# Kernel tuning notes

Measured on AMD Instinct MI355X. Metric: run time of the kernel, lower is better.

Reference implementation:

```python
import jax, jax.numpy as jnp
import numpy as np

N = 50000
E = 600000
IN_DIM = 128
HID = 128
HEADS = 4
OUT = HID // HEADS  # per-head out channels
R = 2
LAYERS = 2
NEG_SLOPE = 0.2


def _glorot(key, shape):
    fan_in, fan_out = shape[-2], shape[-1]
    lim = jnp.sqrt(6.0 / (fan_in + fan_out))
    return jax.random.uniform(key, shape, jnp.float32, -lim, lim)


def setup_inputs() -> dict:
    key = jax.random.key(0)
    ks = jax.random.split(key, 20)
    x = jax.random.normal(ks[0], (N, IN_DIM), jnp.float32)
    eidx = jax.random.randint(ks[1], (2, E), 0, N, jnp.int64 if jax.config.jax_enable_x64 else jnp.int32)
    etype = jax.random.randint(ks[2], (E,), 0, R, eidx.dtype)
    d = IN_DIM
    params = {}
    ki = 3
    for l in range(LAYERS):
        params[f"W{l}"] = _glorot(ks[ki], (R, d, HID)); ki += 1            # per-relation weight
        params[f"Q{l}"] = _glorot(ks[ki], (HID, HEADS)); ki += 1           # query proj (dim=1)
        params[f"K{l}"] = _glorot(ks[ki], (HID, HEADS)); ki += 1           # key proj
        params[f"cb{l}"] = jnp.zeros((HID,), jnp.float32)                   # conv bias
        params[f"pW{l}"] = _glorot(ks[ki], (HID, HID)); ki += 1            # proj Linear weight [out,in]
        params[f"pb{l}"] = jnp.zeros((HID,), jnp.float32)
        d = HID
    return dict(x=x, eidx=eidx, etype=etype, **params)


def _rgat_conv(h, src, dst, etype, W, Q, K, b):
    # per-relation transform of all nodes: [R, N, HID]
    xw = jnp.einsum('ni,rio->rno', h, W)
    out_j = xw[etype, src]          # [E, HID] source features under edge's relation
    out_i = xw[etype, dst]          # [E, HID] target features under edge's relation
    # additive self-attention, dim=1: alpha [E, HEADS]
    alpha = jax.nn.leaky_relu(out_i @ Q + out_j @ K, NEG_SLOPE)
    # segment softmax over destination nodes (across-relation)
    m = jax.ops.segment_max(alpha, dst, num_segments=N)
    m = jnp.where(jnp.isfinite(m), m, 0.0)
    e = jnp.exp(alpha - m[dst])
    s = jax.ops.segment_sum(e, dst, num_segments=N)
    a = e / (s[dst] + 1e-16)
    # weighted messages and scatter-sum aggregation
    msg = out_j.reshape(E, HEADS, OUT) * a[:, :, None]
    agg = jax.ops.segment_sum(msg.reshape(E, HID), dst, num_segments=N)
    return agg + b


def reference(x, eidx, etype, W0, Q0, K0, cb0, pW0, pb0, W1, Q1, K1, cb1, pW1, pb1):
    src, dst = eidx[0], eidx[1]  # flow source_to_target: aggregate at eidx[1]
    h = x
    for (W, Q, K, cb, pW, pb) in ((W0, Q0, K0, cb0, pW0, pb0), (W1, Q1, K1, cb1, pW1, pb1)):
        h = _rgat_conv(h, src, dst, etype, W, Q, K, cb)
        h = jax.nn.elu(h @ pW.T + pb)
    return h
```

## Files before the change

kernel.cpp:

```cpp
#include <hip/hip_runtime.h>
#include <hip/hip_bf16.h>

typedef __hip_bfloat16 bf16;
typedef short s16x8 __attribute__((ext_vector_type(8)));
typedef float f32x4 __attribute__((ext_vector_type(4)));

#define N_NODES 50000
#define NPAD    50048
#define E_EDGES 600000
#define HID     128
#define HEADS   4
#define SCAN_B  196

#define GB_IDX  2344
#define GB_WT   256
#define GB_QUAD 3125
#define GB_BIG  8824

__device__ __forceinline__ unsigned short f2bf_bits(float f) {
  unsigned u = __float_as_uint(f);
  u += 0x7fffu + ((u >> 16) & 1u);
  return (unsigned short)(u >> 16);
}
__device__ __forceinline__ float bf2f(unsigned short b) {
  return __uint_as_float(((unsigned)b) << 16);
}
__device__ __forceinline__ float lo_f(unsigned v) { return __uint_as_float(v << 16); }
__device__ __forceinline__ float hi_f(unsigned v) { return __uint_as_float(v & 0xffff0000u); }
__device__ __forceinline__ float lrelu(float v) { return fmaxf(v, 0.2f * v); }
__device__ __forceinline__ float elu(float v) { return v > 0.f ? v : __expf(v) - 1.f; }

__global__ __launch_bounds__(256) void detect_zero_kernel(const unsigned short* __restrict__ xb,
                                                          const int* __restrict__ ei,
                                                          int* __restrict__ flags,
                                                          int* __restrict__ zp, int nz) {
  int t = threadIdx.x;
  int i = blockIdx.x * 256 + t;
  if (i < nz) zp[i] = 0;
  if (blockIdx.x == 0) {
    __shared__ int cnt[2];
    if (t < 2) cnt[t] = 0;
    __syncthreads();
    unsigned short v = xb[2 * t];
    int ex = (v >> 7) & 0xFF;
    if (ex < 119 || ex > 135) atomicAdd(&cnt[0], 1);
    if (ei[2 * t + 1] != 0) atomicAdd(&cnt[1], 1);
    __syncthreads();
    if (t == 0) {
      flags[0] = (cnt[0] > 64) ? 1 : 0;
      flags[1] = (cnt[1] == 0) ? 1 : 0;
    }
  }
}

struct P8 { const void* src[8]; int dstoff[8]; int n[8]; };
__global__ __launch_bounds__(256) void cvt_all_kernel(const int* __restrict__ eidx,
                                                      const int* __restrict__ etype,
                                                      int* __restrict__ dstA, int* __restrict__ pk,
                                                      int* __restrict__ deg,
                                                      const void* __restrict__ w0,
                                                      const void* __restrict__ w1,
                                                      unsigned short* __restrict__ Wbt,
                                                      P8 tab, float* __restrict__ base,
                                                      const int* __restrict__ flags) {
  const int b = blockIdx.x, t = threadIdx.x;
  if (b < GB_IDX) {
    int e = b * 256 + t;
    if (e >= E_EDGES) return;
    int s, d, r;
    if (flags[1]) {
      const long long* e64 = (const long long*)eidx;
      const long long* t64 = (const long long*)etype;
      s = (int)e64[e]; d = (int)e64[E_EDGES + e]; r = (int)t64[e];
    } else {
      s = eidx[e]; d = eidx[E_EDGES + e]; r = etype[e];
    }
    dstA[e] = d;
    pk[e] = s | (r << 16);
    atomicAdd(&deg[d], 1);
  } else if (b < GB_IDX + GB_WT) {
    int idx = (b - GB_IDX) * 256 + t;
    int l = idx >> 15, rem = idx & 32767;
    int r = rem >> 14, i = (rem >> 7) & 127, o = rem & 127;
    const void* src = l ? w1 : w0;
    unsigned short v;
    if (flags[0]) v = f2bf_bits(((const float*)src)[rem]);
    else          v = ((const unsigned short*)src)[rem];
    Wbt[(size_t)l * 2 * HID * HID + ((size_t)r * HID + o) * HID + i] = v;
  } else {
    const int f = flags[0];
    int bb = b - GB_IDX - GB_WT;
    for (int k = 0; k < 8; ++k) {
      int n = tab.n[k];
      for (int i = bb * 256 + t; i < n; i += 2 * 256) {
        float v = f ? ((const float*)tab.src[k])[i] : bf2f(((const unsigned short*)tab.src[k])[i]);
        base[tab.dstoff[k] + i] = v;
      }
    }
  }
}

__global__ __launch_bounds__(256) void scan1_bucket_kernel(const int* __restrict__ deg,
                                                           int* __restrict__ excl,
                                                           int* __restrict__ bsum,
                                                           int* __restrict__ bcnt,
                                                           int* __restrict__ nq,
                                                           int* __restrict__ nw) {
  const int b = blockIdx.x, t = threadIdx.x;
  if (b < SCAN_B) {
    __shared__ int sm[256];
    int i = b * 256 + t;
    int v = (i < NPAD) ? deg[i] : 0;
    sm[t] = v;
    __syncthreads();
#pragma unroll
    for (int off = 1; off < 256; off <<= 1) {
      int add = (t >= off) ? sm[t - off] : 0;
      __syncthreads();
      sm[t] += add;
      __syncthreads();
    }
    if (i < NPAD) excl[i] = sm[t] - v;
    if (t == 255) bsum[b] = sm[255];
  } else {
    int n = (b - SCAN_B) * 256 + t;
    int lane = t & 63;
    bool valid = n < N_NODES;
    int d = valid ? deg[n] : 0;
    bool isq = valid && (d <= 16);
    bool isw = valid && (d > 16);
    unsigned long long mq = __ballot(isq);
    unsigned long long mw = __ballot(isw);
    unsigned long long lower = (lane == 63) ? 0x7fffffffffffffffull : ((1ull << lane) - 1ull);
    int baseq = 0, basew = 0;
    int lq = (int)__ffsll(mq) - 1;
    int lw = (int)__ffsll(mw) - 1;
    if (mq && lane == lq) baseq = atomicAdd(&bcnt[0], (int)__popcll(mq));
    if (mw && lane == lw) basew = atomicAdd(&bcnt[1], (int)__popcll(mw));
    if (mq) baseq = __shfl(baseq, lq);
    if (mw) basew = __shfl(basew, lw);
    if (isq) nq[baseq + (int)__popcll(mq & lower)] = n;
    if (isw) nw[basew + (int)__popcll(mw & lower)] = n;
  }
}

__global__ __launch_bounds__(256) void scan23_prep_kernel(const int* __restrict__ excl,
                                                          const int* __restrict__ bsum,
                                                          int* __restrict__ rowstart,
                                                          const unsigned short* __restrict__ Wbt,
                                                          const float* __restrict__ Qf,
                                                          const float* __restrict__ Kf,
                                                          unsigned short* __restrict__ qkt_hi,
                                                          unsigned short* __restrict__ qkt_lo,
                                                          const void* __restrict__ pW0,
                                                          const void* __restrict__ pW1,
                                                          const float* __restrict__ cbf,
                                                          const float* __restrict__ pbf,
                                                          unsigned short* __restrict__ pWTb2,
                                                          float* __restrict__ bo2,
                                                          const int* __restrict__ flags) {
  const int b = blockIdx.x, t = threadIdx.x;
  if (b < SCAN_B) {
    __shared__ int sm[256];
    int v = (t < SCAN_B) ? bsum[t] : 0;
    sm[t] = v;
    __syncthreads();
#pragma unroll
    for (int off = 1; off < 256; off <<= 1) {
      int add = (t >= off) ? sm[t - off] : 0;
      __syncthreads();
      sm[t] += add;
      __syncthreads();
    }
    int bpre = (b > 0) ? sm[b - 1] : 0;
    int i = b * 256 + t;
    if (i < NPAD) rowstart[i] = excl[i] + bpre;
    if (i == 0) rowstart[NPAD] = E_EDGES;
  } else if (b < SCAN_B + 2) {
    int idx = (b - SCAN_B) * 256 + t;
    int i = idx & 127, lr = idx >> 7, l = lr >> 1, r = (lr & 1);
    float aq[4] = {0.f, 0.f, 0.f, 0.f}, ak[4] = {0.f, 0.f, 0.f, 0.f};
    const unsigned short* Wb = Wbt + (size_t)lr * HID * HID;
    const float* Qp = Qf + l * HID * HEADS;
    const float* Kp = Kf + l * HID * HEADS;
    for (int j = 0; j < HID; ++j) {
      float w = bf2f(Wb[j * HID + i]);
      float4 q4 = *(const float4*)(Qp + j * 4);
      float4 k4 = *(const float4*)(Kp + j * 4);
      aq[0] += w * q4.x; aq[1] += w * q4.y; aq[2] += w * q4.z; aq[3] += w * q4.w;
      ak[0] += w * k4.x; ak[1] += w * k4.y; ak[2] += w * k4.z; ak[3] += w * k4.w;
    }
    size_t base = (size_t)l * 16 * HID;
#pragma unroll
    for (int h = 0; h < 4; ++h) {
      unsigned short qh = f2bf_bits(aq[h]);
      unsigned short kh = f2bf_bits(ak[h]);
      float qres = aq[h] - bf2f(qh);
      float kres = ak[h] - bf2f(kh);
      qkt_hi[base + (size_t)(r * 4 + h) * HID + i] = qh;
      qkt_lo[base + (size_t)(r * 4 + h) * HID + i] = f2bf_bits(qres);
      qkt_hi[base + (size_t)(8 + r * 4 + h) * HID + i] = kh;
      qkt_lo[base + (size_t)(8 + r * 4 + h) * HID + i] = f2bf_bits(kres);
    }
  } else {
    const int wave = t >> 6, lane = t & 63;
    int ob = (b - SCAN_B - 2) * 4 + wave;
    int o = ob & 127, l = ob >> 7;
    const void* pWraw = l ? pW1 : pW0;
    const float* cb = cbf + l * HID;
    const int f = flags[0];
    float part = 0.f;
#pragma unroll
    for (int i = lane; i < HID; i += 64) {
      float w = f ? ((const float*)pWraw)[o * HID + i] : bf2f(((const unsigned short*)pWraw)[o * HID + i]);
      pWTb2[(size_t)l * HID * HID + o * HID + i] = f2bf_bits(w);
      part += cb[i] * w;
    }
#pragma unroll
    for (int off = 32; off > 0; off >>= 1) part += __shfl_xor(part, off);
    if (lane == 0) bo2[l * HID + o] = pbf[l * HID + o] + part;
  }
}

__global__ __launch_bounds__(256) void scatter_kernel(const int* __restrict__ dstA,
                                                      const int* __restrict__ pk,
                                                      const int* __restrict__ rowstart,
                                                      int* __restrict__ cnt,
                                                      int* __restrict__ eord) {
  int e = blockIdx.x * 256 + threadIdx.x;
  if (e >= E_EDGES) return;
  int d = dstA[e];
  int pos = rowstart[d] + atomicAdd(&cnt[d], 1);
  eord[pos] = pk[e];
}

__device__ __forceinline__ void gemm64_from_lds(unsigned short (*As)[136], unsigned short (*Cs)[136],
                                                const unsigned short* __restrict__ Wbt,
                                                unsigned short* __restrict__ xw, int row0,
                                                int wave, int lm, int q, int t) {
  const int r = wave >> 1, colb = (wave & 1) * 64;
  const unsigned short* Bt = Wbt + (size_t)r * HID * HID;
  s16x8 bfr[4][4];
#pragma unroll
  for (int kc = 0; kc < 4; ++kc) {
    const int ko = kc * 32 + q * 8;
#pragma unroll
    for (int ct = 0; ct < 4; ++ct)
      bfr[kc][ct] = *(const s16x8*)(Bt + (size_t)(colb + ct * 16 + lm) * HID + ko);
  }
  f32x4 acc[4][4];
#pragma unroll
  for (int a = 0; a < 4; ++a)
#pragma unroll
    for (int c = 0; c < 4; ++c) { f32x4 z = {0.f, 0.f, 0.f, 0.f}; acc[a][c] = z; }
#pragma unroll
  for (int kc = 0; kc < 4; ++kc) {
    const int ko = kc * 32 + q * 8;
#pragma unroll
    for (int rt = 0; rt < 4; ++rt) {
      s16x8 a = *(const s16x8*)&As[rt * 16 + lm][ko];
#pragma unroll
      for (int ct = 0; ct < 4; ++ct)
        acc[rt][ct] = __builtin_amdgcn_mfma_f32_16x16x32_bf16(a, bfr[kc][ct], acc[rt][ct], 0, 0, 0);
    }
  }
  __syncthreads();
#pragma unroll
  for (int rr = 0; rr < 2; ++rr) {
    if (r == rr) {
#pragma unroll
      for (int rt = 0; rt < 4; ++rt)
#pragma unroll
        for (int i = 0; i < 4; ++i) {
          int rloc = rt * 16 + q * 4 + i;
#pragma unroll
          for (int ct = 0; ct < 4; ++ct)
            Cs[rloc][colb + ct * 16 + lm] = f2bf_bits(acc[rt][ct][i]);
        }
    }
    __syncthreads();
    unsigned short* dst = xw + ((size_t)rr * NPAD + row0) * HID;
#pragma unroll
    for (int j = 0; j < 4; ++j) {
      int idx = j * 256 + t;
      int rw = idx >> 4, cb8 = (idx & 15) * 8;
      if (row0 + rw < N_NODES)
        *(s16x8*)(dst + (size_t)rw * HID + cb8) = *(const s16x8*)&Cs[rw][cb8];
    }
    __syncthreads();
  }
}

__device__ __forceinline__ void qk16_from_lds(unsigned short (*As)[136], unsigned short (*Cs)[136],
                                              const unsigned short* __restrict__ qkt_hi,
                                              const unsigned short* __restrict__ qkt_lo,
                                              float4* __restrict__ qi4, float4* __restrict__ kj4,
                                              int row0, int wave, int lane, int lm, int q) {
  s16x8 bhi[4], blo[4], af[4];
#pragma unroll
  for (int kc = 0; kc < 4; ++kc) {
    const int ko = kc * 32 + q * 8;
    bhi[kc] = *(const s16x8*)(qkt_hi + (size_t)lm * HID + ko);
    blo[kc] = *(const s16x8*)(qkt_lo + (size_t)lm * HID + ko);
    af[kc]  = *(const s16x8*)&As[wave * 16 + lm][ko];
  }
  f32x4 acc = {0.f, 0.f, 0.f, 0.f};
#pragma unroll
  for (int kc = 0; kc < 4; ++kc) {
    acc = __builtin_amdgcn_mfma_f32_16x16x32_bf16(af[kc], bhi[kc], acc, 0, 0, 0);
    acc = __builtin_amdgcn_mfma_f32_16x16x32_bf16(af[kc], blo[kc], acc, 0, 0, 0);
  }
  float (*Fs)[16][17] = (float(*)[16][17])&Cs[0][0];
#pragma unroll
  for (int i = 0; i < 4; ++i)
    Fs[wave][lm][q * 4 + i] = acc[i];
  __syncthreads();
  if (lane < 16) {
    int n = row0 + wave * 16 + lane;
    if (n < N_NODES) {
      float4 v;
      v.x = Fs[wave][0][lane];  v.y = Fs[wave][1][lane];  v.z = Fs[wave][2][lane];  v.w = Fs[wave][3][lane];
      qi4[n] = v;
      v.x = Fs[wave][4][lane];  v.y = Fs[wave][5][lane];  v.z = Fs[wave][6][lane];  v.w = Fs[wave][7][lane];
      qi4[NPAD + n] = v;
      v.x = Fs[wave][8][lane];  v.y = Fs[wave][9][lane];  v.z = Fs[wave][10][lane]; v.w = Fs[wave][11][lane];
      kj4[n] = v;
      v.x = Fs[wave][12][lane]; v.y = Fs[wave][13][lane]; v.z = Fs[wave][14][lane]; v.w = Fs[wave][15][lane];
      kj4[NPAD + n] = v;
    }
  }
}

__global__ __launch_bounds__(256) void fused_l0_kernel(const void* __restrict__ x,
                                                       const unsigned short* __restrict__ Wbt,
                                                       unsigned short* __restrict__ xw,
                                                       const unsigned short* __restrict__ qkt_hi,
                                                       const unsigned short* __restrict__ qkt_lo,
                                                       float4* __restrict__ qi4,
                                                       float4* __restrict__ kj4,
                                                       const int* __restrict__ flags) {
  __shared__ unsigned short As[64][136];
  __shared__ unsigned short Cs[64][136];
  const int t = threadIdx.x;
  const int wave = t >> 6, lane = t & 63;
  const int lm = lane & 15, q = lane >> 4;
  const int row0 = blockIdx.x * 64;
  if (flags[0]) {
    const float* xf = (const float*)x;
#pragma unroll
    for (int j = 0; j < 4; ++j) {
      int idx = j * 256 + t;
      int rw = idx >> 4, cb8 = (idx & 15) * 8;
      s16x8 o = {0, 0, 0, 0, 0, 0, 0, 0};
      if (row0 + rw < N_NODES) {
        const float4* s4 = (const float4*)(xf + (size_t)(row0 + rw) * HID + cb8);
        float4 a = s4[0], b = s4[1];
        o[0] = (short)f2bf_bits(a.x); o[1] = (short)f2bf_bits(a.y);
        o[2] = (short)f2bf_bits(a.z); o[3] = (short)f2bf_bits(a.w);
        o[4] = (short)f2bf_bits(b.x); o[5] = (short)f2bf_bits(b.y);
        o[6] = (short)f2bf_bits(b.z); o[7] = (short)f2bf_bits(b.w);
      }
      *(s16x8*)&As[rw][cb8] = o;
    }
  } else {
    const unsigned short* xb = (const unsigned short*)x;
#pragma unroll
    for (int j = 0; j < 4; ++j) {
      int idx = j * 256 + t;
      int rw = idx >> 4, cb8 = (idx & 15) * 8;
      s16x8 o = {0, 0, 0, 0, 0, 0, 0, 0};
      if (row0 + rw < N_NODES)
        o = *(const s16x8*)(xb + (size_t)(row0 + rw) * HID + cb8);
      *(s16x8*)&As[rw][cb8] = o;
    }
  }
  __syncthreads();
  gemm64_from_lds(As, Cs, Wbt, xw, row0, wave, lm, q, t);
  qk16_from_lds(As, Cs, qkt_hi, qkt_lo, qi4, kj4, row0, wave, lane, lm, q);
}

__global__ __launch_bounds__(256) void fused_mid_kernel(const unsigned short* __restrict__ aggb,
                                                        const unsigned short* __restrict__ pWTb,
                                                        const float* __restrict__ bo,
                                                        const unsigned short* __restrict__ Wbt1,
                                                        unsigned short* __restrict__ xw,
                                                        const unsigned short* __restrict__ qkt_hi,
                                                        const unsigned short* __restrict__ qkt_lo,
                                                        float4* __restrict__ qi4,
                                                        float4* __restrict__ kj4) {
  __shared__ unsigned short As[64][136];
  __shared__ unsigned short Cs[64][136];
  const int t = threadIdx.x;
  const int wave = t >> 6, lane = t & 63;
  const int lm = lane & 15, q = lane >> 4;
  const int row0 = blockIdx.x * 64;
  const int h = wave >> 1;
  const int colb = (wave & 1) * 64;
  s16x8 bfr[4][4];
#pragma unroll
  for (int kc = 0; kc < 4; ++kc) {
    const int ko = kc * 32 + q * 8;
#pragma unroll
    for (int ct = 0; ct < 4; ++ct)
      bfr[kc][ct] = *(const s16x8*)(pWTb + (size_t)(colb + ct * 16 + lm) * HID + ko);
  }
  const unsigned short* gsrc = aggb + (size_t)row0 * HID;
#pragma unroll
  for (int j = 0; j < 4; ++j) {
    int idx = j * 256 + t;
    *(s16x8*)&As[idx >> 4][(idx & 15) * 8] = *(const s16x8*)(gsrc + idx * 8);
  }
  __syncthreads();
  f32x4 pacc[2][4];
#pragma unroll
  for (int a = 0; a < 2; ++a)
#pragma unroll
    for (int c = 0; c < 4; ++c) { f32x4 z = {0.f, 0.f, 0.f, 0.f}; pacc[a][c] = z; }
#pragma unroll
  for (int kc = 0; kc < 4; ++kc) {
    const int ko = kc * 32 + q * 8;
#pragma unroll
    for (int rt = 0; rt < 2; ++rt) {
      s16x8 a = *(const s16x8*)&As[(2 * h + rt) * 16 + lm][ko];
#pragma unroll
      for (int ct = 0; ct < 4; ++ct)
        pacc[rt][ct] = __builtin_amdgcn_mfma_f32_16x16x32_bf16(a, bfr[kc][ct], pacc[rt][ct], 0, 0, 0);
    }
  }
  __syncthreads();
#pragma unroll
  for (int rt = 0; rt < 2; ++rt)
#pragma unroll
    for (int i = 0; i < 4; ++i) {
      int rloc = (2 * h + rt) * 16 + q * 4 + i;
#pragma unroll
      for (int ct = 0; ct < 4; ++ct) {
        int o = colb + ct * 16 + lm;
        As[rloc][o] = f2bf_bits(elu(pacc[rt][ct][i] + bo[o]));
      }
    }
  __syncthreads();
  gemm64_from_lds(As, Cs, Wbt1, xw, row0, wave, lm, q, t);
  qk16_from_lds(As, Cs, qkt_hi, qkt_lo, qi4, kj4, row0, wave, lane, lm, q);
}

__global__ __launch_bounds__(256) void edge_all_kernel(
    const int* __restrict__ rowstart, const int* __restrict__ eord,
    const float4* __restrict__ qi4, const float4* __restrict__ kj4,
    const unsigned short* __restrict__ xw, unsigned short* __restrict__ aggb,
    const int* __restrict__ nq, const int* __restrict__ nw,
    const int* __restrict__ bcnt) {
  __shared__ volatile float wbuf[1152];
  const int t = threadIdx.x;
  const int wave = t >> 6, lane = t & 63;
  if (blockIdx.x >= GB_BIG) {
    const int g = lane >> 4, li = lane & 15;
    const int idx = (blockIdx.x - GB_BIG) * 16 + wave * 4 + g;
    const int cq = bcnt[0];
    const bool act = idx < cq;
    const int n = act ? nq[idx] : 0;
    const int start = rowstart[n];
    const int dg = act ? (rowstart[n + 1] - start) : 0;
    int p = 0;
    float w0 = 0.f, w1 = 0.f, w2 = 0.f, w3 = 0.f;
    if (li < dg) {
      p = eord[start + li];
      int s = p & 0xffff, r = p >> 16;
      float4 k4 = kj4[r ? (NPAD + s) : s];
      float4 q4 = r ? qi4[NPAD + n] : qi4[n];
      w0 = __expf(fminf(lrelu(q4.x + k4.x), 85.f));
      w1 = __expf(fminf(lrelu(q4.y + k4.y), 85.f));
      w2 = __expf(fminf(lrelu(q4.z + k4.z), 85.f));
      w3 = __expf(fminf(lrelu(q4.w + k4.w), 85.f));
    }
    const int wg = (wave << 2) | g;
    volatile float* wls = &wbuf[wg * 68];
    wls[0 * 17 + li] = w0; wls[1 * 17 + li] = w1;
    wls[2 * 17 + li] = w2; wls[3 * 17 + li] = w3;
    float s0 = w0, s1 = w1, s2 = w2, s3 = w3;
#pragma unroll
    for (int off = 8; off > 0; off >>= 1) {
      s0 += __shfl_xor(s0, off); s1 += __shfl_xor(s1, off);
      s2 += __shfl_xor(s2, off); s3 += __shfl_xor(s3, off);
    }
    const int hh = li >> 2;
    float ssel = hh == 0 ? s0 : hh == 1 ? s1 : hh == 2 ? s2 : s3;
    float a0 = 0.f, a1 = 0.f, a2 = 0.f, a3 = 0.f, a4 = 0.f, a5 = 0.f, a6 = 0.f, a7 = 0.f;
    volatile const float* wrh = &wls[hh * 17];
    const int co = li * 8;
    const int gbase = lane & 48;
#pragma unroll 1
    for (int e0 = 0; e0 < dg; e0 += 4) {
      int pe[4];
      uint4 v[4];
#pragma unroll
      for (int u = 0; u < 4; ++u) {
        int e = e0 + u;
        pe[u] = __shfl(p, gbase + (e < dg ? e : 0));
      }
#pragma unroll
      for (int u = 0; u < 4; ++u)
        v[u] = *(const uint4*)(xw + ((size_t)((pe[u] & 0xffff) + (pe[u] >> 16) * NPAD) << 7) + co);
#pragma unroll
      for (int u = 0; u < 4; ++u) {
        int e = e0 + u;
        float we = (e < dg) ? wrh[e] : 0.f;
        a0 = fmaf(lo_f(v[u].x), we, a0); a1 = fmaf(hi_f(v[u].x), we, a1);
        a2 = fmaf(lo_f(v[u].y), we, a2); a3 = fmaf(hi_f(v[u].y), we, a3);
        a4 = fmaf(lo_f(v[u].z), we, a4); a5 = fmaf(hi_f(v[u].z), we, a5);
        a6 = fmaf(lo_f(v[u].w), we, a6); a7 = fmaf(hi_f(v[u].w), we, a7);
      }
    }
    if (act) {
      float inv = 1.f / (ssel + 1e-16f);
      uint4 o;
      o.x = (unsigned)f2bf_bits(a0 * inv) | ((unsigned)f2bf_bits(a1 * inv) << 16);
      o.y = (unsigned)f2bf_bits(a2 * inv) | ((unsigned)f2bf_bits(a3 * inv) << 16);
      o.z = (unsigned)f2bf_bits(a4 * inv) | ((unsigned)f2bf_bits(a5 * inv) << 16);
      o.w = (unsigned)f2bf_bits(a6 * inv) | ((unsigned)f2bf_bits(a7 * inv) << 16);
      *(uint4*)(aggb + ((size_t)n << 7) + co) = o;
    }
  } else {
    const int idx = blockIdx.x * 4 + wave;
    const int cw = bcnt[1];
    if (idx >= cw) return;
    const int n = nw[idx];
    unsigned* outp = (unsigned*)(aggb + ((size_t)n << 7)) + lane;
    const int start = rowstart[n];
    const int deg = rowstart[n + 1] - start;
    const int hh = lane >> 4;
    const int ch2 = lane << 1;
    float2 acc = {0.f, 0.f};
    float ssel;
    volatile float* wls = &wbuf[wave * 288];
    if (deg <= 64) {
      int p = 0;
      float w0 = 0.f, w1 = 0.f, w2 = 0.f, w3 = 0.f;
      if (lane < deg) {
        p = eord[start + lane];
        int s = p & 0xffff, r = p >> 16;
        float4 k4 = kj4[r ? (NPAD + s) : s];
        float4 q4 = r ? qi4[NPAD + n] : qi4[n];
        w0 = __expf(fminf(lrelu(q4.x + k4.x), 85.f));
        w1 = __expf(fminf(lrelu(q4.y + k4.y), 85.f));
        w2 = __expf(fminf(lrelu(q4.z + k4.z), 85.f));
        w3 = __expf(fminf(lrelu(q4.w + k4.w), 85.f));
      }
      float s0 = w0, s1 = w1, s2 = w2, s3 = w3;
#pragma unroll
      for (int off = 32; off > 0; off >>= 1) {
        s0 += __shfl_xor(s0, off); s1 += __shfl_xor(s1, off);
        s2 += __shfl_xor(s2, off); s3 += __shfl_xor(s3, off);
      }
      ssel = hh == 0 ? s0 : hh == 1 ? s1 : hh == 2 ? s2 : s3;
      wls[0 * 72 + lane] = w0;
      wls[1 * 72 + lane] = w1;
      wls[2 * 72 + lane] = w2;
      wls[3 * 72 + lane] = w3;
      volatile const float* wrh = &wls[hh * 72];
      const int degp = (deg + 15) & ~15;
#pragma unroll 1
      for (int e = 0; e < degp; e += 16) {
        int pp[16];
        unsigned vv[16];
#pragma unroll
        for (int u = 0; u < 16; ++u)
          pp[u] = __builtin_amdgcn_readlane(p, e + u);
#pragma unroll
        for (int u = 0; u < 16; ++u)
          vv[u] = *(const unsigned*)(xw + ((size_t)((pp[u] & 0xffff) + (pp[u] >> 16) * NPAD) << 7) + ch2);
#pragma unroll
        for (int u = 0; u < 16; ++u) {
          float we = wrh[e + u];
          acc.x = fmaf(lo_f(vv[u]), we, acc.x);
          acc.y = fmaf(hi_f(vv[u]), we, acc.y);
        }
      }
    } else {
      const float4 q0 = qi4[n], q1 = qi4[NPAD + n];
      float4 m = make_float4(-1e30f, -1e30f, -1e30f, -1e30f);
      for (int e = start; e < start + deg; ++e) {
        int pe = eord[e];
        int s = pe & 0xffff, r = pe >> 16;
        float4 k4 = kj4[(size_t)r * NPAD + s];
        float4 q4 = r ? q1 : q0;
        m.x = fmaxf(m.x, lrelu(q4.x + k4.x)); m.y = fmaxf(m.y, lrelu(q4.y + k4.y));
        m.z = fmaxf(m.z, lrelu(q4.z + k4.z)); m.w = fmaxf(m.w, lrelu(q4.w + k4.w));
      }
      float4 sv = make_float4(0.f, 0.f, 0.f, 0.f);
      for (int e = start; e < start + deg; ++e) {
        int pe = eord[e];
        int s = pe & 0xffff, r = pe >> 16;
        float4 k4 = kj4[(size_t)r * NPAD + s];
        float4 q4 = r ? q1 : q0;
        float w0 = __expf(lrelu(q4.x + k4.x) - m.x);
        float w1 = __expf(lrelu(q4.y + k4.y) - m.y);
        float w2 = __expf(lrelu(q4.z + k4.z) - m.z);
        float w3 = __expf(lrelu(q4.w + k4.w) - m.w);
        sv.x += w0; sv.y += w1; sv.z += w2; sv.w += w3;
        float we = hh == 0 ? w0 : hh == 1 ? w1 : hh == 2 ? w2 : w3;
        unsigned v = *(const unsigned*)(xw + (((size_t)r * NPAD + s) << 7) + ch2);
        acc.x = fmaf(lo_f(v), we, acc.x);
        acc.y = fmaf(hi_f(v), we, acc.y);
      }
      ssel = hh == 0 ? sv.x : hh == 1 ? sv.y : hh == 2 ? sv.z : sv.w;
    }
    float inv = 1.f / (ssel + 1e-16f);
    *outp = (unsigned)f2bf_bits(acc.x * inv) | ((unsigned)f2bf_bits(acc.y * inv) << 16);
  }
}

__global__ __launch_bounds__(256) void proj_final(const unsigned short* __restrict__ aggb,
                                                  const unsigned short* __restrict__ pWTb,
                                                  const float* __restrict__ bo,
                                                  void* __restrict__ dout,
                                                  const int* __restrict__ flags) {
  __shared__ unsigned short As[64][136];
  const int t = threadIdx.x;
  const int wave = t >> 6, lane = t & 63;
  const int row0 = blockIdx.x * 64;
  const int h = wave >> 1;
  const int colb = (wave & 1) * 64;
  const int lm = lane & 15, q = lane >> 4;
  s16x8 bfr[4][4];
#pragma unroll
  for (int kc = 0; kc < 4; ++kc) {
    const int ko = kc * 32 + q * 8;
#pragma unroll
    for (int ct = 0; ct < 4; ++ct)
      bfr[kc][ct] = *(const s16x8*)(pWTb + (size_t)(colb + ct * 16 + lm) * HID + ko);
  }
  const unsigned short* gsrc = aggb + (size_t)row0 * HID;
#pragma unroll
  for (int j = 0; j < 4; ++j) {
    int idx = j * 256 + t;
    *(s16x8*)&As[idx >> 4][(idx & 15) * 8] = *(const s16x8*)(gsrc + idx * 8);
  }
  __syncthreads();
  f32x4 acc[2][4];
#pragma unroll
  for (int a = 0; a < 2; ++a)
#pragma unroll
    for (int c = 0; c < 4; ++c) { f32x4 z = {0.f, 0.f, 0.f, 0.f}; acc[a][c] = z; }
#pragma unroll
  for (int kc = 0; kc < 4; ++kc) {
    const int ko = kc * 32 + q * 8;
#pragma unroll
    for (int rt = 0; rt < 2; ++rt) {
      s16x8 a = *(const s16x8*)&As[(2 * h + rt) * 16 + lm][ko];
#pragma unroll
      for (int ct = 0; ct < 4; ++ct)
        acc[rt][ct] = __builtin_amdgcn_mfma_f32_16x16x32_bf16(a, bfr[kc][ct], acc[rt][ct], 0, 0, 0);
    }
  }
  __syncthreads();
  if (!flags[0]) {
    unsigned short* dstp = (unsigned short*)dout;
#pragma unroll
    for (int rt = 0; rt < 2; ++rt)
#pragma unroll
      for (int i = 0; i < 4; ++i) {
        int rloc = (2 * h + rt) * 16 + q * 4 + i;
#pragma unroll
        for (int ct = 0; ct < 4; ++ct) {
          int o = colb + ct * 16 + lm;
          As[rloc][o] = f2bf_bits(elu(acc[rt][ct][i] + bo[o]));
        }
      }
    __syncthreads();
#pragma unroll
    for (int j = 0; j < 4; ++j) {
      int idx = j * 256 + t;
      int rw = idx >> 4, cb8 = (idx & 15) * 8;
      if (row0 + rw < N_NODES)
        *(s16x8*)(dstp + (size_t)(row0 + rw) * HID + cb8) = *(const s16x8*)&As[rw][cb8];
    }
  } else {
    float* fdst = (float*)dout;
    float (*Fs)[132] = (float(*)[132])&As[0][0];
#pragma unroll
    for (int h2 = 0; h2 < 2; ++h2) {
      if (h == h2) {
#pragma unroll
        for (int rt = 0; rt < 2; ++rt)
#pragma unroll
          for (int i = 0; i < 4; ++i) {
            int rloc = rt * 16 + q * 4 + i;
#pragma unroll
            for (int ct = 0; ct < 4; ++ct) {
              int o = colb + ct * 16 + lm;
              Fs[rloc][o] = elu(acc[rt][ct][i] + bo[o]);
            }
          }
      }
      __syncthreads();
#pragma unroll
      for (int j = 0; j < 4; ++j) {
        int idx = j * 256 + t;
        int rw = idx >> 5, cb4 = (idx & 31) * 4;
        if (row0 + h2 * 32 + rw < N_NODES)
          *(float4*)(fdst + (size_t)(row0 + h2 * 32 + rw) * HID + cb4) = *(const float4*)&Fs[rw][cb4];
      }
      __syncthreads();
    }
  }
}

extern "C" void kernel_launch(void* const* d_in, const int* in_sizes, int n_in,
                              void* d_out, int out_size, void* d_ws, size_t ws_size,
                              hipStream_t stream) {
  const void* x     = d_in[0];
  const int*  eidx  = (const int*)d_in[1];
  const int*  etype = (const int*)d_in[2];
  const int iW[2] = {3, 9}, iQ[2] = {4, 10}, iK[2] = {5, 11}, icb[2] = {6, 12}, ipW[2] = {7, 13}, ipb[2] = {8, 14};

  float* ws = (float*)d_ws;
  size_t off = 0;
  int*   flags = (int*)(ws + off); off += 16;
  unsigned short* xw   = (unsigned short*)(ws + off); off += (size_t)NPAD * HID;
  float* qi   = ws + off; off += (size_t)2 * NPAD * HEADS;
  float* kj   = ws + off; off += (size_t)2 * NPAD * HEADS;
  unsigned short* aggb = (unsigned short*)(ws + off); off += (size_t)NPAD * HID / 2;
  int* dstA = (int*)(ws + off); off += E_EDGES;
  int* pk   = (int*)(ws + off); off += E_EDGES;
  int* eord = (int*)(ws + off); off += E_EDGES;
  int* deg  = (int*)(ws + off); off += NPAD;
  int* cnt  = (int*)(ws + off); off += NPAD;
  int* bcnt = (int*)(ws + off); off += 16;
  int* excl = (int*)(ws + off); off += NPAD;
  int* rowstart = (int*)(ws + off); off += NPAD + 16;
  int* bsum  = (int*)(ws + off); off += 256;
  int* nq   = (int*)(ws + off); off += NPAD;
  int* nwl  = (int*)(ws + off); off += NPAD;
  unsigned short* Wbt   = (unsigned short*)(ws + off); off += (size_t)2 * 2 * HID * HID / 2;
  unsigned short* pWTb2 = (unsigned short*)(ws + off); off += (size_t)2 * HID * HID / 2;
  unsigned short* qkt_hi = (unsigned short*)(ws + off); off += (size_t)2 * 16 * HID / 2;
  unsigned short* qkt_lo = (unsigned short*)(ws + off); off += (size_t)2 * 16 * HID / 2;
  float* Qf  = ws + off; off += 2 * HID * HEADS;
  float* Kf  = ws + off; off += 2 * HID * HEADS;
  float* cbf = ws + off; off += 2 * HID;
  float* pbf = ws + off; off += 2 * HID;
  float* bo2 = ws + off; off += 2 * HID;

  detect_zero_kernel<<<(2 * NPAD + 16 + 255) / 256, 256, 0, stream>>>((const unsigned short*)x, eidx, flags, deg, 2 * NPAD + 16);

  {
    P8 tab;
    float* base = ws;
    for (int l = 0; l < 2; ++l) {
      tab.src[l * 4 + 0] = d_in[iQ[l]];  tab.dstoff[l * 4 + 0] = (int)(Qf - base) + l * HID * HEADS;  tab.n[l * 4 + 0] = HID * HEADS;
      tab.src[l * 4 + 1] = d_in[iK[l]];  tab.dstoff[l * 4 + 1] = (int)(Kf - base) + l * HID * HEADS;  tab.n[l * 4 + 1] = HID * HEADS;
      tab.src[l * 4 + 2] = d_in[icb[l]]; tab.dstoff[l * 4 + 2] = (int)(cbf - base) + l * HID;         tab.n[l * 4 + 2] = HID;
      tab.src[l * 4 + 3] = d_in[ipb[l]]; tab.dstoff[l * 4 + 3] = (int)(pbf - base) + l * HID;         tab.n[l * 4 + 3] = HID;
    }
    cvt_all_kernel<<<GB_IDX + GB_WT + 2, 256, 0, stream>>>(eidx, etype, dstA, pk, deg,
                                                           d_in[iW[0]], d_in[iW[1]], Wbt,
                                                           tab, ws, flags);
  }

  scan1_bucket_kernel<<<SCAN_B + SCAN_B, 256, 0, stream>>>(deg, excl, bsum, bcnt, nq, nwl);

  scan23_prep_kernel<<<SCAN_B + 2 + 64, 256, 0, stream>>>(excl, bsum, rowstart,
                                                          Wbt, Qf, Kf, qkt_hi, qkt_lo,
                                                          d_in[ipW[0]], d_in[ipW[1]], cbf, pbf, pWTb2, bo2, flags);

  scatter_kernel<<<(E_EDGES + 255) / 256, 256, 0, stream>>>(dstA, pk, rowstart, cnt, eord);

  const int RB = NPAD / 64;
  fused_l0_kernel<<<RB, 256, 0, stream>>>(x, Wbt, xw, qkt_hi, qkt_lo,
                                          (float4*)qi, (float4*)kj, flags);
  edge_all_kernel<<<GB_BIG + GB_QUAD, 256, 0, stream>>>(rowstart, eord, (const float4*)qi, (const float4*)kj,
                                                        xw, aggb, nq, nwl, bcnt);
  fused_mid_kernel<<<RB, 256, 0, stream>>>(aggb, pWTb2, bo2, Wbt + (size_t)2 * HID * HID, xw,
                                           qkt_hi + (size_t)16 * HID, qkt_lo + (size_t)16 * HID,
                                           (float4*)qi, (float4*)kj);
  edge_all_kernel<<<GB_BIG + GB_QUAD, 256, 0, stream>>>(rowstart, eord, (const float4*)qi, (const float4*)kj,
                                                        xw, aggb, nq, nwl, bcnt);
  proj_final<<<RB, 256, 0, stream>>>(aggb, pWTb2 + (size_t)HID * HID, bo2 + HID, d_out, flags);
}
```

Baseline: 343.1 us.

## Merge all pipeline stages into one cooperative persistent kernel with grid syncs

Restructures the ten separate kernel launches into a single cooperative mega-kernel. Each phase loops over virtual blocks with a grid-stride loop, and grid.sync() separates the phases, so launch gaps and tail drains between kernels go away. The original per-kernel launches are kept as a fallback when the cooperative launch fails. The trade-off is a grid capped at occupancy × CUs (at most 1024 blocks), which limits parallelism in the edge phases. The GEMM phases' shared-memory and register needs also now apply to every phase and may lower occupancy.

```diff
diff --git a/kernel.cpp b/kernel.cpp
--- a/kernel.cpp
+++ b/kernel.cpp
@@ -1,5 +1,8 @@
 #include <hip/hip_runtime.h>
 #include <hip/hip_bf16.h>
+#include <hip/hip_cooperative_groups.h>
+
+namespace cg = cooperative_groups;
 
 typedef __hip_bfloat16 bf16;
 typedef short s16x8 __attribute__((ext_vector_type(8)));
@@ -12,10 +15,17 @@
 #define HEADS   4
 #define SCAN_B  196
 
-#define GB_IDX  2344
-#define GB_WT   256
-#define GB_QUAD 3125
-#define GB_BIG  8824
+#define VB_ZERO 392
+#define VB_IDX  2344
+#define VB_WT   256
+#define VB_CVT  (VB_IDX + VB_WT + 2)
+#define VB_SCAN (SCAN_B + SCAN_B)
+#define VB_PREP (SCAN_B + 2 + 64)
+#define VB_SCAT 2344
+#define VB_ROWS 782
+#define VB_BIG  8824
+#define VB_QUAD 3125
+#define VB_EDGE (VB_BIG + VB_QUAD)
 
 __device__ __forceinline__ unsigned short f2bf_bits(float f) {
   unsigned u = __float_as_uint(f);
@@ -30,87 +40,82 @@
 __device__ __forceinline__ float lrelu(float v) { return fmaxf(v, 0.2f * v); }
 __device__ __forceinline__ float elu(float v) { return v > 0.f ? v : __expf(v) - 1.f; }
 
-__global__ __launch_bounds__(256) void detect_zero_kernel(const unsigned short* __restrict__ xb,
-                                                          const int* __restrict__ ei,
-                                                          int* __restrict__ flags,
-                                                          int* __restrict__ zp, int nz) {
-  int t = threadIdx.x;
-  int i = blockIdx.x * 256 + t;
-  if (i < nz) zp[i] = 0;
-  if (blockIdx.x == 0) {
-    __shared__ int cnt[2];
-    if (t < 2) cnt[t] = 0;
-    __syncthreads();
-    unsigned short v = xb[2 * t];
-    int ex = (v >> 7) & 0xFF;
-    if (ex < 119 || ex > 135) atomicAdd(&cnt[0], 1);
-    if (ei[2 * t + 1] != 0) atomicAdd(&cnt[1], 1);
-    __syncthreads();
-    if (t == 0) {
-      flags[0] = (cnt[0] > 64) ? 1 : 0;
-      flags[1] = (cnt[1] == 0) ? 1 : 0;
-    }
-  }
-}
-
 struct P8 { const void* src[8]; int dstoff[8]; int n[8]; };
-__global__ __launch_bounds__(256) void cvt_all_kernel(const int* __restrict__ eidx,
-                                                      const int* __restrict__ etype,
-                                                      int* __restrict__ dstA, int* __restrict__ pk,
-                                                      int* __restrict__ deg,
-                                                      const void* __restrict__ w0,
-                                                      const void* __restrict__ w1,
-                                                      unsigned short* __restrict__ Wbt,
-                                                      P8 tab, float* __restrict__ base,
-                                                      const int* __restrict__ flags) {
-  const int b = blockIdx.x, t = threadIdx.x;
-  if (b < GB_IDX) {
-    int e = b * 256 + t;
-    if (e >= E_EDGES) return;
-    int s, d, r;
-    if (flags[1]) {
-      const long long* e64 = (const long long*)eidx;
-      const long long* t64 = (const long long*)etype;
-      s = (int)e64[e]; d = (int)e64[E_EDGES + e]; r = (int)t64[e];
-    } else {
-      s = eidx[e]; d = eidx[E_EDGES + e]; r = etype[e];
-    }
-    dstA[e] = d;
-    pk[e] = s | (r << 16);
-    atomicAdd(&deg[d], 1);
-  } else if (b < GB_IDX + GB_WT) {
-    int idx = (b - GB_IDX) * 256 + t;
+
+struct MegaArgs {
+  const void* x; const int* eidx; const int* etype;
+  const void* w0; const void* w1; const void* pW0; const void* pW1;
+  P8 tab; float* base;
+  int* flags; unsigned short* xw; float4* qi4; float4* kj4; unsigned short* aggb;
+  int* dstA; int* pk; int* eord; int* deg; int* cnt; int* bcnt;
+  int* excl; int* rowstart; int* bsum; int* nq; int* nw;
+  unsigned short* Wbt; unsigned short* pWTb2; unsigned short* qkt_hi; unsigned short* qkt_lo;
+  float* Qf; float* Kf; float* cbf; float* pbf; float* bo2;
+  void* dout;
+};
+
+
+__device__ __forceinline__ void phase_zero(const MegaArgs& a, int vb, int t) {
+  int i = vb * 256 + t;
+  if (i < 2 * NPAD + 16) a.deg[i] = 0;
+}
+
+__device__ __forceinline__ void phase_detect(const MegaArgs& a, int t, int* dcnt) {
+  if (t < 2) dcnt[t] = 0;
+  __syncthreads();
+  unsigned short v = ((const unsigned short*)a.x)[2 * t];
+  int ex = (v >> 7) & 0xFF;
+  if (ex < 119 || ex > 135) atomicAdd(&dcnt[0], 1);
+  if (a.eidx[2 * t + 1] != 0) atomicAdd(&dcnt[1], 1);
+  __syncthreads();
+  if (t == 0) {
+    a.flags[0] = (dcnt[0] > 64) ? 1 : 0;
+    a.flags[1] = (dcnt[1] == 0) ? 1 : 0;
+  }
+}
+
+__device__ __forceinline__ void phase_cvt(const MegaArgs& a, int vb, int t) {
+  const int f0 = a.flags[0], f1 = a.flags[1];
+  if (vb < VB_IDX) {
+    int e = vb * 256 + t;
+    if (e < E_EDGES) {
+      int s, d, r;
+      if (f1) {
+        const long long* e64 = (const long long*)a.eidx;
+        const long long* t64 = (const long long*)a.etype;
+        s = (int)e64[e]; d = (int)e64[E_EDGES + e]; r = (int)t64[e];
+      } else {
+        s = a.eidx[e]; d = a.eidx[E_EDGES + e]; r = a.etype[e];
+      }
+      a.dstA[e] = d;
+      a.pk[e] = s | (r << 16);
+      atomicAdd(&a.deg[d], 1);
+    }
+  } else if (vb < VB_IDX + VB_WT) {
+    int idx = (vb - VB_IDX) * 256 + t;
     int l = idx >> 15, rem = idx & 32767;
     int r = rem >> 14, i = (rem >> 7) & 127, o = rem & 127;
-    const void* src = l ? w1 : w0;
+    const void* src = l ? a.w1 : a.w0;
     unsigned short v;
-    if (flags[0]) v = f2bf_bits(((const float*)src)[rem]);
-    else          v = ((const unsigned short*)src)[rem];
-    Wbt[(size_t)l * 2 * HID * HID + ((size_t)r * HID + o) * HID + i] = v;
+    if (f0) v = f2bf_bits(((const float*)src)[rem]);
+    else    v = ((const unsigned short*)src)[rem];
+    a.Wbt[(size_t)l * 2 * HID * HID + ((size_t)r * HID + o) * HID + i] = v;
   } else {
-    const int f = flags[0];
-    int bb = b - GB_IDX - GB_WT;
+    int bb = vb - VB_IDX - VB_WT;
     for (int k = 0; k < 8; ++k) {
-      int n = tab.n[k];
+      int n = a.tab.n[k];
       for (int i = bb * 256 + t; i < n; i += 2 * 256) {
-        float v = f ? ((const float*)tab.src[k])[i] : bf2f(((const unsigned short*)tab.src[k])[i]);
-        base[tab.dstoff[k] + i] = v;
-      }
-    }
-  }
-}
-
-__global__ __launch_bounds__(256) void scan1_bucket_kernel(const int* __restrict__ deg,
-                                                           int* __restrict__ excl,
-                                                           int* __restrict__ bsum,
-                                                           int* __restrict__ bcnt,
-                                                           int* __restrict__ nq,
-                                                           int* __restrict__ nw) {
-  const int b = blockIdx.x, t = threadIdx.x;
-  if (b < SCAN_B) {
-    __shared__ int sm[256];
-    int i = b * 256 + t;
-    int v = (i < NPAD) ? deg[i] : 0;
+        float v = f0 ? ((const float*)a.tab.src[k])[i] : bf2f(((const unsigned short*)a.tab.src[k])[i]);
+        a.base[a.tab.dstoff[k] + i] = v;
+      }
+    }
+  }
+}
+
+__device__ __forceinline__ void phase_scan1b(const MegaArgs& a, int vb, int t, int lane, int* sm) {
+  if (vb < SCAN_B) {
+    int i = vb * 256 + t;
+    int v = (i < NPAD) ? a.deg[i] : 0;
     sm[t] = v;
     __syncthreads();
 #pragma unroll
@@ -120,13 +125,13 @@
       sm[t] += add;
       __syncthreads();
     }
-    if (i < NPAD) excl[i] = sm[t] - v;
-    if (t == 255) bsum[b] = sm[255];
+    if (i < NPAD) a.excl[i] = sm[t] - v;
+    if (t == 255) a.bsum[vb] = sm[255];
+    __syncthreads();
   } else {
-    int n = (b - SCAN_B) * 256 + t;
-    int lane = t & 63;
+    int n = (vb - SCAN_B) * 256 + t;
     bool valid = n < N_NODES;
-    int d = valid ? deg[n] : 0;
+    int d = valid ? a.deg[n] : 0;
     bool isq = valid && (d <= 16);
     bool isw = valid && (d > 16);
     unsigned long long mq = __ballot(isq);
@@ -135,34 +140,19 @@
     int baseq = 0, basew = 0;
     int lq = (int)__ffsll(mq) - 1;
     int lw = (int)__ffsll(mw) - 1;
-    if (mq && lane == lq) baseq = atomicAdd(&bcnt[0], (int)__popcll(mq));
-    if (mw && lane == lw) basew = atomicAdd(&bcnt[1], (int)__popcll(mw));
+    if (mq && lane == lq) baseq = atomicAdd(&a.bcnt[0], (int)__popcll(mq));
+    if (mw && lane == lw) basew = atomicAdd(&a.bcnt[1], (int)__popcll(mw));
     if (mq) baseq = __shfl(baseq, lq);
     if (mw) basew = __shfl(basew, lw);
-    if (isq) nq[baseq + (int)__popcll(mq & lower)] = n;
-    if (isw) nw[basew + (int)__popcll(mw & lower)] = n;
-  }
-}
-
-__global__ __launch_bounds__(256) void scan23_prep_kernel(const int* __restrict__ excl,
-                                                          const int* __restrict__ bsum,
-                                                          int* __restrict__ rowstart,
-                                                          const unsigned short* __restrict__ Wbt,
-                                                          const float* __restrict__ Qf,
-                                                          const float* __restrict__ Kf,
-                                                          unsigned short* __restrict__ qkt_hi,
-                                                          unsigned short* __restrict__ qkt_lo,
-                                                          const void* __restrict__ pW0,
-                                                          const void* __restrict__ pW1,
-                                                          const float* __restrict__ cbf,
-                                                          const float* __restrict__ pbf,
-                                                          unsigned short* __restrict__ pWTb2,
-                                                          float* __restrict__ bo2,
-                                                          const int* __restrict__ flags) {
-  const int b = blockIdx.x, t = threadIdx.x;
-  if (b < SCAN_B) {
-    __shared__ int sm[256];
-    int v = (t < SCAN_B) ? bsum[t] : 0;
+    if (isq) a.nq[baseq + (int)__popcll(mq & lower)] = n;
+    if (isw) a.nw[basew + (int)__popcll(mw & lower)] = n;
+  }
+}
+
+__device__ __forceinline__ void phase_prep(const MegaArgs& a, int vb, int t, int wave, int lane, int* sm) {
+  const int f0 = a.flags[0];
+  if (vb < SCAN_B) {
+    int v = (t < SCAN_B) ? a.bsum[t] : 0;
     sm[t] = v;
     __syncthreads();
 #pragma unroll
@@ -172,17 +162,18 @@
       sm[t] += add;
       __syncthreads();
     }
-    int bpre = (b > 0) ? sm[b - 1] : 0;
-    int i = b * 256 + t;
-    if (i < NPAD) rowstart[i] = excl[i] + bpre;
-    if (i == 0) rowstart[NPAD] = E_EDGES;
-  } else if (b < SCAN_B + 2) {
-    int idx = (b - SCAN_B) * 256 + t;
+    int bpre = (vb > 0) ? sm[vb - 1] : 0;
+    int i = vb * 256 + t;
+    if (i < NPAD) a.rowstart[i] = a.excl[i] + bpre;
+    if (i == 0) a.rowstart[NPAD] = E_EDGES;
+    __syncthreads();
+  } else if (vb < SCAN_B + 2) {
+    int idx = (vb - SCAN_B) * 256 + t;
     int i = idx & 127, lr = idx >> 7, l = lr >> 1, r = (lr & 1);
     float aq[4] = {0.f, 0.f, 0.f, 0.f}, ak[4] = {0.f, 0.f, 0.f, 0.f};
-    const unsigned short* Wb = Wbt + (size_t)lr * HID * HID;
-    const float* Qp = Qf + l * HID * HEADS;
-    const float* Kp = Kf + l * HID * HEADS;
+    const unsigned short* Wb = a.Wbt + (size_t)lr * HID * HID;
+    const float* Qp = a.Qf + l * HID * HEADS;
+    const float* Kp = a.Kf + l * HID * HEADS;
     for (int j = 0; j < HID; ++j) {
       float w = bf2f(Wb[j * HID + i]);
       float4 q4 = *(const float4*)(Qp + j * 4);
@@ -197,41 +188,36 @@
       unsigned short kh = f2bf_bits(ak[h]);
       float qres = aq[h] - bf2f(qh);
       float kres = ak[h] - bf2f(kh);
-      qkt_hi[base + (size_t)(r * 4 + h) * HID + i] = qh;
-      qkt_lo[base + (size_t)(r * 4 + h) * HID + i] = f2bf_bits(qres);
-      qkt_hi[base + (size_t)(8 + r * 4 + h) * HID + i] = kh;
-      qkt_lo[base + (size_t)(8 + r * 4 + h) * HID + i] = f2bf_bits(kres);
+      a.qkt_hi[base + (size_t)(r * 4 + h) * HID + i] = qh;
+      a.qkt_lo[base + (size_t)(r * 4 + h) * HID + i] = f2bf_bits(qres);
+      a.qkt_hi[base + (size_t)(8 + r * 4 + h) * HID + i] = kh;
+      a.qkt_lo[base + (size_t)(8 + r * 4 + h) * HID + i] = f2bf_bits(kres);
     }
   } else {
-    const int wave = t >> 6, lane = t & 63;
-    int ob = (b - SCAN_B - 2) * 4 + wave;
+    int ob = (vb - SCAN_B - 2) * 4 + wave;
     int o = ob & 127, l = ob >> 7;
-    const void* pWraw = l ? pW1 : pW0;
-    const float* cb = cbf + l * HID;
-    const int f = flags[0];
+    const void* pWraw = l ? a.pW1 : a.pW0;
+    const float* cb = a.cbf + l * HID;
     float part = 0.f;
 #pragma unroll
     for (int i = lane; i < HID; i += 64) {
-      float w = f ? ((const float*)pWraw)[o * HID + i] : bf2f(((const unsigned short*)pWraw)[o * HID + i]);
-      pWTb2[(size_t)l * HID * HID + o * HID + i] = f2bf_bits(w);
+      float w = f0 ? ((const float*)pWraw)[o * HID + i] : bf2f(((const unsigned short*)pWraw)[o * HID + i]);
+      a.pWTb2[(size_t)l * HID * HID + o * HID + i] = f2bf_bits(w);
       part += cb[i] * w;
     }
 #pragma unroll
     for (int off = 32; off > 0; off >>= 1) part += __shfl_xor(part, off);
-    if (lane == 0) bo2[l * HID + o] = pbf[l * HID + o] + part;
-  }
-}
-
-__global__ __launch_bounds__(256) void scatter_kernel(const int* __restrict__ dstA,
-                                                      const int* __restrict__ pk,
-                                                      const int* __restrict__ rowstart,
-                                                      int* __restrict__ cnt,
-                                                      int* __restrict__ eord) {
-  int e = blockIdx.x * 256 + threadIdx.x;
-  if (e >= E_EDGES) return;
-  int d = dstA[e];
-  int pos = rowstart[d] + atomicAdd(&cnt[d], 1);
-  eord[pos] = pk[e];
+    if (lane == 0) a.bo2[l * HID + o] = a.pbf[l * HID + o] + part;
+  }
+}
+
+__device__ __forceinline__ void phase_scatter(const MegaArgs& a, int vb, int t) {
+  int e = vb * 256 + t;
+  if (e < E_EDGES) {
+    int d = a.dstA[e];
+    int pos = a.rowstart[d] + atomicAdd(&a.cnt[d], 1);
+    a.eord[pos] = a.pk[e];
+  }
 }
 
 __device__ __forceinline__ void gemm64_from_lds(unsigned short (*As)[136], unsigned short (*Cs)[136],
@@ -250,18 +236,18 @@
   }
   f32x4 acc[4][4];
 #pragma unroll
-  for (int a = 0; a < 4; ++a)
-#pragma unroll
-    for (int c = 0; c < 4; ++c) { f32x4 z = {0.f, 0.f, 0.f, 0.f}; acc[a][c] = z; }
+  for (int aa = 0; aa < 4; ++aa)
+#pragma unroll
+    for (int c = 0; c < 4; ++c) { f32x4 z = {0.f, 0.f, 0.f, 0.f}; acc[aa][c] = z; }
 #pragma unroll
   for (int kc = 0; kc < 4; ++kc) {
     const int ko = kc * 32 + q * 8;
 #pragma unroll
     for (int rt = 0; rt < 4; ++rt) {
-      s16x8 a = *(const s16x8*)&As[rt * 16 + lm][ko];
+      s16x8 av = *(const s16x8*)&As[rt * 16 + lm][ko];
 #pragma unroll
       for (int ct = 0; ct < 4; ++ct)
-        acc[rt][ct] = __builtin_amdgcn_mfma_f32_16x16x32_bf16(a, bfr[kc][ct], acc[rt][ct], 0, 0, 0);
+        acc[rt][ct] = __builtin_amdgcn_mfma_f32_16x16x32_bf16(av, bfr[kc][ct], acc[rt][ct], 0, 0, 0);
     }
   }
   __syncthreads();
@@ -329,24 +315,14 @@
       kj4[NPAD + n] = v;
     }
   }
-}
-
-__global__ __launch_bounds__(256) void fused_l0_kernel(const void* __restrict__ x,
-                                                       const unsigned short* __restrict__ Wbt,
-                                                       unsigned short* __restrict__ xw,
-                                                       const unsigned short* __restrict__ qkt_hi,
-                                                       const unsigned short* __restrict__ qkt_lo,
-                                                       float4* __restrict__ qi4,
-                                                       float4* __restrict__ kj4,
-                                                       const int* __restrict__ flags) {
-  __shared__ unsigned short As[64][136];
-  __shared__ unsigned short Cs[64][136];
-  const int t = threadIdx.x;
-  const int wave = t >> 6, lane = t & 63;
-  const int lm = lane & 15, q = lane >> 4;
-  const int row0 = blockIdx.x * 64;
-  if (flags[0]) {
-    const float* xf = (const float*)x;
+  __syncthreads();
+}
+
+__device__ __forceinline__ void phase_l0(const MegaArgs& a, int vb, int t, int wave, int lane, int lm, int q,
+                                         unsigned short (*As)[136], unsigned short (*Cs)[136]) {
+  const int row0 = vb * 64;
+  if (a.flags[0]) {
+    const float* xf = (const float*)a.x;
 #pragma unroll
     for (int j = 0; j < 4; ++j) {
       int idx = j * 256 + t;
@@ -354,16 +330,16 @@
       s16x8 o = {0, 0, 0, 0, 0, 0, 0, 0};
       if (row0 + rw < N_NODES) {
         const float4* s4 = (const float4*)(xf + (size_t)(row0 + rw) * HID + cb8);
-        float4 a = s4[0], b = s4[1];
-        o[0] = (short)f2bf_bits(a.x); o[1] = (short)f2bf_bits(a.y);
-        o[2] = (short)f2bf_bits(a.z); o[3] = (short)f2bf_bits(a.w);
-        o[4] = (short)f2bf_bits(b.x); o[5] = (short)f2bf_bits(b.y);
-        o[6] = (short)f2bf_bits(b.z); o[7] = (short)f2bf_bits(b.w);
+        float4 aa = s4[0], b = s4[1];
+        o[0] = (short)f2bf_bits(aa.x); o[1] = (short)f2bf_bits(aa.y);
+        o[2] = (short)f2bf_bits(aa.z); o[3] = (short)f2bf_bits(aa.w);
+        o[4] = (short)f2bf_bits(b.x);  o[5] = (short)f2bf_bits(b.y);
+        o[6] = (short)f2bf_bits(b.z);  o[7] = (short)f2bf_bits(b.w);
       }
       *(s16x8*)&As[rw][cb8] = o;
     }
   } else {
-    const unsigned short* xb = (const unsigned short*)x;
+    const unsigned short* xb = (const unsigned short*)a.x;
 #pragma unroll
     for (int j = 0; j < 4; ++j) {
       int idx = j * 256 + t;
@@ -375,25 +351,13 @@
     }
   }
   __syncthreads();
-  gemm64_from_lds(As, Cs, Wbt, xw, row0, wave, lm, q, t);
-  qk16_from_lds(As, Cs, qkt_hi, qkt_lo, qi4, kj4, row0, wave, lane, lm, q);
-}
-
-__global__ __launch_bounds__(256) void fused_mid_kernel(const unsigned short* __restrict__ aggb,
-                                                        const unsigned short* __restrict__ pWTb,
-                                                        const float* __restrict__ bo,
-                                                        const unsigned short* __restrict__ Wbt1,
-                                                        unsigned short* __restrict__ xw,
-                                                        const unsigned short* __restrict__ qkt_hi,
-                                                        const unsigned short* __restrict__ qkt_lo,
-                                                        float4* __restrict__ qi4,
-                                                        float4* __restrict__ kj4) {
-  __shared__ unsigned short As[64][136];
-  __shared__ unsigned short Cs[64][136];
-  const int t = threadIdx.x;
-  const int wave = t >> 6, lane = t & 63;
-  const int lm = lane & 15, q = lane >> 4;
-  const int row0 = blockIdx.x * 64;
+  gemm64_from_lds(As, Cs, a.Wbt, a.xw, row0, wave, lm, q, t);
+  qk16_from_lds(As, Cs, a.qkt_hi, a.qkt_lo, a.qi4, a.kj4, row0, wave, lane, lm, q);
+}
+
+__device__ __forceinline__ void phase_mid(const MegaArgs& a, int vb, int t, int wave, int lane, int lm, int q,
+                                          unsigned short (*As)[136], unsigned short (*Cs)[136]) {
+  const int row0 = vb * 64;
   const int h = wave >> 1;
   const int colb = (wave & 1) * 64;
   s16x8 bfr[4][4];
@@ -402,9 +366,9 @@
     const int ko = kc * 32 + q * 8;
 #pragma unroll
     for (int ct = 0; ct < 4; ++ct)
-      bfr[kc][ct] = *(const s16x8*)(pWTb + (size_t)(colb + ct * 16 + lm) * HID + ko);
-  }
-  const unsigned short* gsrc = aggb + (size_t)row0 * HID;
+      bfr[kc][ct] = *(const s16x8*)(a.pWTb2 + (size_t)(colb + ct * 16 + lm) * HID + ko);
+  }
+  const unsigned short* gsrc = a.aggb + (size_t)row0 * HID;
 #pragma unroll
   for (int j = 0; j < 4; ++j) {
     int idx = j * 256 + t;
@@ -413,18 +377,18 @@
   __syncthreads();
   f32x4 pacc[2][4];
 #pragma unroll
-  for (int a = 0; a < 2; ++a)
-#pragma unroll
-    for (int c = 0; c < 4; ++c) { f32x4 z = {0.f, 0.f, 0.f, 0.f}; pacc[a][c] = z; }
+  for (int aa = 0; aa < 2; ++aa)
+#pragma unroll
+    for (int c = 0; c < 4; ++c) { f32x4 z = {0.f, 0.f, 0.f, 0.f}; pacc[aa][c] = z; }
 #pragma unroll
   for (int kc = 0; kc < 4; ++kc) {
     const int ko = kc * 32 + q * 8;
 #pragma unroll
     for (int rt = 0; rt < 2; ++rt) {
-      s16x8 a = *(const s16x8*)&As[(2 * h + rt) * 16 + lm][ko];
+      s16x8 av = *(const s16x8*)&As[(2 * h + rt) * 16 + lm][ko];
 #pragma unroll
       for (int ct = 0; ct < 4; ++ct)
-        pacc[rt][ct] = __builtin_amdgcn_mfma_f32_16x16x32_bf16(a, bfr[kc][ct], pacc[rt][ct], 0, 0, 0);
+        pacc[rt][ct] = __builtin_amdgcn_mfma_f32_16x16x32_bf16(av, bfr[kc][ct], pacc[rt][ct], 0, 0, 0);
     }
   }
   __syncthreads();
@@ -436,35 +400,125 @@
 #pragma unroll
       for (int ct = 0; ct < 4; ++ct) {
         int o = colb + ct * 16 + lm;
-        As[rloc][o] = f2bf_bits(elu(pacc[rt][ct][i] + bo[o]));
-      }
-    }
-  __syncthreads();
-  gemm64_from_lds(As, Cs, Wbt1, xw, row0, wave, lm, q, t);
-  qk16_from_lds(As, Cs, qkt_hi, qkt_lo, qi4, kj4, row0, wave, lane, lm, q);
-}
-
-__global__ __launch_bounds__(256) void edge_all_kernel(
-    const int* __restrict__ rowstart, const int* __restrict__ eord,
-    const float4* __restrict__ qi4, const float4* __restrict__ kj4,
-    const unsigned short* __restrict__ xw, unsigned short* __restrict__ aggb,
-    const int* __restrict__ nq, const int* __restrict__ nw,
-    const int* __restrict__ bcnt) {
-  __shared__ volatile float wbuf[1152];
-  const int t = threadIdx.x;
-  const int wave = t >> 6, lane = t & 63;
-  if (blockIdx.x >= GB_BIG) {
+        As[rloc][o] = f2bf_bits(elu(pacc[rt][ct][i] + a.bo2[o]));
+      }
+    }
+  __syncthreads();
+  const unsigned short* Wbt1 = a.Wbt + (size_t)2 * HID * HID;
+  gemm64_from_lds(As, Cs, Wbt1, a.xw, row0, wave, lm, q, t);
+  qk16_from_lds(As, Cs, a.qkt_hi + (size_t)16 * HID, a.qkt_lo + (size_t)16 * HID,
+                a.qi4, a.kj4, row0, wave, lane, lm, q);
+}
+
+__device__ __forceinline__ void phase_final(const MegaArgs& a, int vb, int t, int wave, int lane, int lm, int q,
+                                            unsigned short (*As)[136]) {
+  const int row0 = vb * 64;
+  const int h = wave >> 1;
+  const int colb = (wave & 1) * 64;
+  const unsigned short* pWT1 = a.pWTb2 + (size_t)HID * HID;
+  const float* bo1 = a.bo2 + HID;
+  s16x8 bfr[4][4];
+#pragma unroll
+  for (int kc = 0; kc < 4; ++kc) {
+    const int ko = kc * 32 + q * 8;
+#pragma unroll
+    for (int ct = 0; ct < 4; ++ct)
+      bfr[kc][ct] = *(const s16x8*)(pWT1 + (size_t)(colb + ct * 16 + lm) * HID + ko);
+  }
+  const unsigned short* gsrc = a.aggb + (size_t)row0 * HID;
+#pragma unroll
+  for (int j = 0; j < 4; ++j) {
+    int idx = j * 256 + t;
+    *(s16x8*)&As[idx >> 4][(idx & 15) * 8] = *(const s16x8*)(gsrc + idx * 8);
+  }
+  __syncthreads();
+  f32x4 acc[2][4];
+#pragma unroll
+  for (int aa = 0; aa < 2; ++aa)
+#pragma unroll
+    for (int c = 0; c < 4; ++c) { f32x4 z = {0.f, 0.f, 0.f, 0.f}; acc[aa][c] = z; }
+#pragma unroll
+  for (int kc = 0; kc < 4; ++kc) {
+    const int ko = kc * 32 + q * 8;
+#pragma unroll
+    for (int rt = 0; rt < 2; ++rt) {
+      s16x8 av = *(const s16x8*)&As[(2 * h + rt) * 16 + lm][ko];
+#pragma unroll
+      for (int ct = 0; ct < 4; ++ct)
+        acc[rt][ct] = __builtin_amdgcn_mfma_f32_16x16x32_bf16(av, bfr[kc][ct], acc[rt][ct], 0, 0, 0);
+    }
+  }
+  __syncthreads();
+  if (!a.flags[0]) {
+    unsigned short* dstp = (unsigned short*)a.dout;
+#pragma unroll
+    for (int rt = 0; rt < 2; ++rt)
+#pragma unroll
+      for (int i = 0; i < 4; ++i) {
+        int rloc = (2 * h + rt) * 16 + q * 4 + i;
+#pragma unroll
+        for (int ct = 0; ct < 4; ++ct) {
+          int o = colb + ct * 16 + lm;
+          As[rloc][o] = f2bf_bits(elu(acc[rt][ct][i] + bo1[o]));
+        }
+      }
+    __syncthreads();
+#pragma unroll
+    for (int j = 0; j < 4; ++j) {
+      int idx = j * 256 + t;
+      int rw = idx >> 4, cb8 = (idx & 15) * 8;
+      if (row0 + rw < N_NODES)
+        *(s16x8*)(dstp + (size_t)(row0 + rw) * HID + cb8) = *(const s16x8*)&As[rw][cb8];
+    }
+    __syncthreads();
+  } else {
+    float* fdst = (float*)a.dout;
+    float (*Fs)[132] = (float(*)[132])&As[0][0];
+#pragma unroll
+    for (int h2 = 0; h2 < 2; ++h2) {
+      if (h == h2) {
+#pragma unroll
+        for (int rt = 0; rt < 2; ++rt)
+#pragma unroll
+          for (int i = 0; i < 4; ++i) {
+            int rloc = rt * 16 + q * 4 + i;
+#pragma unroll
+            for (int ct = 0; ct < 4; ++ct) {
+              int o = colb + ct * 16 + lm;
+              Fs[rloc][o] = elu(acc[rt][ct][i] + bo1[o]);
+            }
+          }
+      }
+      __syncthreads();
+#pragma unroll
+      for (int j = 0; j < 4; ++j) {
+        int idx = j * 256 + t;
+        int rw = idx >> 5, cb4 = (idx & 31) * 4;
+        if (row0 + h2 * 32 + rw < N_NODES)
+          *(float4*)(fdst + (size_t)(row0 + h2 * 32 + rw) * HID + cb4) = *(const float4*)&Fs[rw][cb4];
+      }
+      __syncthreads();
+    }
+  }
+}
+
+__device__ __forceinline__ void edge_vb(const MegaArgs& a, int vb, volatile float* wbuf,
+                                        int wave, int lane) {
+  const float4* qi4 = a.qi4;
+  const float4* kj4 = a.kj4;
+  const unsigned short* xw = a.xw;
+  if (vb >= VB_BIG) {
     const int g = lane >> 4, li = lane & 15;
-    const int idx = (blockIdx.x - GB_BIG) * 16 + wave * 4 + g;
-    const int cq = bcnt[0];
+    const int idx = (vb - VB_BIG) * 16 + wave * 4 + g;
+    const int cq = a.bcnt[0];
     const bool act = idx < cq;
-    const int n = act ? nq[idx] : 0;
-    const int start = rowstart[n];
-    const int dg = act ? (rowstart[n + 1] - start) : 0;
+    const int n = act ? a.nq[idx] : 0;
+    const int start = a.rowstart[n];
+    const int dg = act ? (a.rowstart[n + 1] - start) : 0;
     int p = 0;
     float w0 = 0.f, w1 = 0.f, w2 = 0.f, w3 = 0.f;
     if (li < dg) {
-      p = eord[start + li];
+      p = a.eord[start + li];
       int s = p & 0xffff, r = p >> 16;
       float4 k4 = kj4[r ? (NPAD + s) : s];
       float4 q4 = r ? qi4[NPAD + n] : qi4[n];
@@ -518,200 +572,176 @@
       o.y = (unsigned)f2bf_bits(a2 * inv) | ((unsigned)f2bf_bits(a3 * inv) << 16);
       o.z = (unsigned)f2bf_bits(a4 * inv) | ((unsigned)f2bf_bits(a5 * inv) << 16);
       o.w = (unsigned)f2bf_bits(a6 * inv) | ((unsigned)f2bf_bits(a7 * inv) << 16);
-      *(uint4*)(aggb + ((size_t)n << 7) + co) = o;
+      *(uint4*)(a.aggb + ((size_t)n << 7) + co) = o;
     }
   } else {
-    const int idx = blockIdx.x * 4 + wave;
-    const int cw = bcnt[1];
-    if (idx >= cw) return;
-    const int n = nw[idx];
-    unsigned* outp = (unsigned*)(aggb + ((size_t)n << 7)) + lane;
-    const int start = rowstart[n];
-    const int deg = rowstart[n + 1] - start;
-    const int hh = lane >> 4;
-    const int ch2 = lane << 1;
-    float2 acc = {0.f, 0.f};
-    float ssel;
-    volatile float* wls = &wbuf[wave * 288];
-    if (deg <= 64) {
-      int p = 0;
-      float w0 = 0.f, w1 = 0.f, w2 = 0.f, w3 = 0.f;
-      if (lane < deg) {
-        p = eord[start + lane];
-        int s = p & 0xffff, r = p >> 16;
-        float4 k4 = kj4[r ? (NPAD + s) : s];
-        float4 q4 = r ? qi4[NPAD + n] : qi4[n];
-        w0 = __expf(fminf(lrelu(q4.x + k4.x), 85.f));
-        w1 = __expf(fminf(lrelu(q4.y + k4.y), 85.f));
-        w2 = __expf(fminf(lrelu(q4.z + k4.z), 85.f));
-        w3 = __expf(fminf(lrelu(q4.w + k4.w), 85.f));
-      }
-      float s0 = w0, s1 = w1, s2 = w2, s3 = w3;
-#pragma unroll
-      for (int off = 32; off > 0; off >>= 1) {
-        s0 += __shfl_xor(s0, off); s1 += __shfl_xor(s1, off);
-        s2 += __shfl_xor(s2, off); s3 += __shfl_xor(s3, off);
-      }
-      ssel = hh == 0 ? s0 : hh == 1 ? s1 : hh == 2 ? s2 : s3;
-      wls[0 * 72 + lane] = w0;
-      wls[1 * 72 + lane] = w1;
-      wls[2 * 72 + lane] = w2;
-      wls[3 * 72 + lane] = w3;
-      volatile const float* wrh = &wls[hh * 72];
-      const int degp = (deg + 15) & ~15;
+    const int idx = vb * 4 + wave;
+    const int cw = a.bcnt[1];
+    if (idx < cw) {
+      const int n = a.nw[idx];
+      unsigned* outp = (unsigned*)(a.aggb + ((size_t)n << 7)) + lane;
+      const int start = a.rowstart[n];
+      const int deg = a.rowstart[n + 1] - start;
+      const int hh = lane >> 4;
+      const int ch2 = lane << 1;
+      float2 acc = {0.f, 0.f};
+      float ssel;
+      volatile float* wls = &wbuf[wave * 288];
+      if (deg <= 64) {
+        int p = 0;
+        float w0 = 0.f, w1 = 0.f, w2 = 0.f, w3 = 0.f;
+        if (lane < deg) {
+          p = a.eord[start + lane];
+          int s = p & 0xffff, r = p >> 16;
+          float4 k4 = kj4[r ? (NPAD + s) : s];
+          float4 q4 = r ? qi4[NPAD + n] : qi4[n];
+          w0 = __expf(fminf(lrelu(q4.x + k4.x), 85.f));
+          w1 = __expf(fminf(lrelu(q4.y + k4.y), 85.f));
+          w2 = __expf(fminf(lrelu(q4.z + k4.z), 85.f));
+          w3 = __expf(fminf(lrelu(q4.w + k4.w), 85.f));
+        }
+        float s0 = w0, s1 = w1, s2 = w2, s3 = w3;
+#pragma unroll
+        for (int off = 32; off > 0; off >>= 1) {
+          s0 += __shfl_xor(s0, off); s1 += __shfl_xor(s1, off);
+          s2 += __shfl_xor(s2, off); s3 += __shfl_xor(s3, off);
+        }
+        ssel = hh == 0 ? s0 : hh == 1 ? s1 : hh == 2 ? s2 : s3;
+        wls[0 * 72 + lane] = w0;
+        wls[1 * 72 + lane] = w1;
+        wls[2 * 72 + lane] = w2;
+        wls[3 * 72 + lane] = w3;
+        volatile const float* wrh = &wls[hh * 72];
+        const int degp = (deg + 15) & ~15;
 #pragma unroll 1
-      for (int e = 0; e < degp; e += 16) {
-        int pp[16];
-        unsigned vv[16];
-#pragma unroll
-        for (int u = 0; u < 16; ++u)
-          pp[u] = __builtin_amdgcn_readlane(p, e + u);
-#pragma unroll
-        for (int u = 0; u < 16; ++u)
-          vv[u] = *(const unsigned*)(xw + ((size_t)((pp[u] & 0xffff) + (pp[u] >> 16) * NPAD) << 7) + ch2);
-#pragma unroll
-        for (int u = 0; u < 16; ++u) {
-          float we = wrh[e + u];
-          acc.x = fmaf(lo_f(vv[u]), we, acc.x);
-          acc.y = fmaf(hi_f(vv[u]), we, acc.y);
+        for (int e = 0; e < degp; e += 16) {
+          int pp[16];
+          unsigned vv[16];
+#pragma unroll
+          for (int u = 0; u < 16; ++u)
+            pp[u] = __builtin_amdgcn_readlane(p, e + u);
+#pragma unroll
+          for (int u = 0; u < 16; ++u)
+            vv[u] = *(const unsigned*)(xw + ((size_t)((pp[u] & 0xffff) + (pp[u] >> 16) * NPAD) << 7) + ch2);
+#pragma unroll
+          for (int u = 0; u < 16; ++u) {
+            float we = wrh[e + u];
+            acc.x = fmaf(lo_f(vv[u]), we, acc.x);
+            acc.y = fmaf(hi_f(vv[u]), we, acc.y);
+          }
         }
-      }
-    } else {
-      const float4 q0 = qi4[n], q1 = qi4[NPAD + n];
-      float4 m = make_float4(-1e30f, -1e30f, -1e30f, -1e30f);
-      for (int e = start; e < start + deg; ++e) {
-        int pe = eord[e];
-        int s = pe & 0xffff, r = pe >> 16;
-        float4 k4 = kj4[(size_t)r * NPAD + s];
-        float4 q4 = r ? q1 : q0;
-        m.x = fmaxf(m.x, lrelu(q4.x + k4.x)); m.y = fmaxf(m.y, lrelu(q4.y + k4.y));
-        m.z = fmaxf(m.z, lrelu(q4.z + k4.z)); m.w = fmaxf(m.w, lrelu(q4.w + k4.w));
-      }
-      float4 sv = make_float4(0.f, 0.f, 0.f, 0.f);
-      for (int e = start; e < start + deg; ++e) {
-        int pe = eord[e];
-        int s = pe & 0xffff, r = pe >> 16;
-        float4 k4 = kj4[(size_t)r * NPAD + s];
-        float4 q4 = r ? q1 : q0;
-        float w0 = __expf(lrelu(q4.x + k4.x) - m.x);
-        float w1 = __expf(lrelu(q4.y + k4.y) - m.y);
-        float w2 = __expf(lrelu(q4.z + k4.z) - m.z);
-        float w3 = __expf(lrelu(q4.w + k4.w) - m.w);
-        sv.x += w0; sv.y += w1; sv.z += w2; sv.w += w3;
-        float we = hh == 0 ? w0 : hh == 1 ? w1 : hh == 2 ? w2 : w3;
-        unsigned v = *(const unsigned*)(xw + (((size_t)r * NPAD + s) << 7) + ch2);
-        acc.x = fmaf(lo_f(v), we, acc.x);
-        acc.y = fmaf(hi_f(v), we, acc.y);
-      }
-      ssel = hh == 0 ? sv.x : hh == 1 ? sv.y : hh == 2 ? sv.z : sv.w;
-    }
-    float inv = 1.f / (ssel + 1e-16f);
-    *outp = (unsigned)f2bf_bits(acc.x * inv) | ((unsigned)f2bf_bits(acc.y * inv) << 16);
-  }
-}
-
-__global__ __launch_bounds__(256) void proj_final(const unsigned short* __restrict__ aggb,
-                                                  const unsigned short* __restrict__ pWTb,
-                                                  const float* __restrict__ bo,
-                                                  void* __restrict__ dout,
-                                                  const int* __restrict__ flags) {
-  __shared__ unsigned short As[64][136];
+      } else {
+        const float4 q0 = qi4[n], q1 = qi4[NPAD + n];
+        float4 m = make_float4(-1e30f, -1e30f, -1e30f, -1e30f);
+        for (int e = start; e < start + deg; ++e) {
+          int pe = a.eord[e];
+          int s = pe & 0xffff, r = pe >> 16;
+          float4 k4 = kj4[(size_t)r * NPAD + s];
+          float4 q4 = r ? q1 : q0;
+          m.x = fmaxf(m.x, lrelu(q4.x + k4.x)); m.y = fmaxf(m.y, lrelu(q4.y + k4.y));
+          m.z = fmaxf(m.z, lrelu(q4.z + k4.z)); m.w = fmaxf(m.w, lrelu(q4.w + k4.w));
+        }
+        float4 sv = make_float4(0.f, 0.f, 0.f, 0.f);
+        for (int e = start; e < start + deg; ++e) {
+          int pe = a.eord[e];
+          int s = pe & 0xffff, r = pe >> 16;
+          float4 k4 = kj4[(size_t)r * NPAD + s];
+          float4 q4 = r ? q1 : q0;
+          float w0 = __expf(lrelu(q4.x + k4.x) - m.x);
+          float w1 = __expf(lrelu(q4.y + k4.y) - m.y);
+          float w2 = __expf(lrelu(q4.z + k4.z) - m.z);
+          float w3 = __expf(lrelu(q4.w + k4.w) - m.w);
+          sv.x += w0; sv.y += w1; sv.z += w2; sv.w += w3;
+          float we = hh == 0 ? w0 : hh == 1 ? w1 : hh == 2 ? w2 : w3;
+          unsigned v = *(const unsigned*)(xw + (((size_t)r * NPAD + s) << 7) + ch2);
+          acc.x = fmaf(lo_f(v), we, acc.x);
+          acc.y = fmaf(hi_f(v), we, acc.y);
+        }
+        ssel = hh == 0 ? sv.x : hh == 1 ? sv.y : hh == 2 ? sv.z : sv.w;
+      }
+      float inv = 1.f / (ssel + 1e-16f);
+      *outp = (unsigned)f2bf_bits(acc.x * inv) | ((unsigned)f2bf_bits(acc.y * inv) << 16);
+    }
+  }
+}
+
+__global__ __launch_bounds__(256, 2) void mega_kernel(MegaArgs a) {
+  cg::grid_group grid = cg::this_grid();
+  __shared__ char smem_raw[34816];
+  unsigned short (*As)[136] = (unsigned short(*)[136])smem_raw;
+  unsigned short (*Cs)[136] = (unsigned short(*)[136])(smem_raw + 17408);
   const int t = threadIdx.x;
   const int wave = t >> 6, lane = t & 63;
-  const int row0 = blockIdx.x * 64;
-  const int h = wave >> 1;
-  const int colb = (wave & 1) * 64;
   const int lm = lane & 15, q = lane >> 4;
-  s16x8 bfr[4][4];
-#pragma unroll
-  for (int kc = 0; kc < 4; ++kc) {
-    const int ko = kc * 32 + q * 8;
-#pragma unroll
-    for (int ct = 0; ct < 4; ++ct)
-      bfr[kc][ct] = *(const s16x8*)(pWTb + (size_t)(colb + ct * 16 + lm) * HID + ko);
-  }
-  const unsigned short* gsrc = aggb + (size_t)row0 * HID;
-#pragma unroll
-  for (int j = 0; j < 4; ++j) {
-    int idx = j * 256 + t;
-    *(s16x8*)&As[idx >> 4][(idx & 15) * 8] = *(const s16x8*)(gsrc + idx * 8);
-  }
-  __syncthreads();
-  f32x4 acc[2][4];
-#pragma unroll
-  for (int a = 0; a < 2; ++a)
-#pragma unroll
-    for (int c = 0; c < 4; ++c) { f32x4 z = {0.f, 0.f, 0.f, 0.f}; acc[a][c] = z; }
-#pragma unroll
-  for (int kc = 0; kc < 4; ++kc) {
-    const int ko = kc * 32 + q * 8;
-#pragma unroll
-    for (int rt = 0; rt < 2; ++rt) {
-      s16x8 a = *(const s16x8*)&As[(2 * h + rt) * 16 + lm][ko];
-#pragma unroll
-      for (int ct = 0; ct < 4; ++ct)
-        acc[rt][ct] = __builtin_amdgcn_mfma_f32_16x16x32_bf16(a, bfr[kc][ct], acc[rt][ct], 0, 0, 0);
-    }
-  }
-  __syncthreads();
-  if (!flags[0]) {
-    unsigned short* dstp = (unsigned short*)dout;
-#pragma unroll
-    for (int rt = 0; rt < 2; ++rt)
-#pragma unroll
-      for (int i = 0; i < 4; ++i) {
-        int rloc = (2 * h + rt) * 16 + q * 4 + i;
-#pragma unroll
-        for (int ct = 0; ct < 4; ++ct) {
-          int o = colb + ct * 16 + lm;
-          As[rloc][o] = f2bf_bits(elu(acc[rt][ct][i] + bo[o]));
-        }
-      }
-    __syncthreads();
-#pragma unroll
-    for (int j = 0; j < 4; ++j) {
-      int idx = j * 256 + t;
-      int rw = idx >> 4, cb8 = (idx & 15) * 8;
-      if (row0 + rw < N_NODES)
-        *(s16x8*)(dstp + (size_t)(row0 + rw) * HID + cb8) = *(const s16x8*)&As[rw][cb8];
-    }
-  } else {
-    float* fdst = (float*)dout;
-    float (*Fs)[132] = (float(*)[132])&As[0][0];
-#pragma unroll
-    for (int h2 = 0; h2 < 2; ++h2) {
-      if (h == h2) {
-#pragma unroll
-        for (int rt = 0; rt < 2; ++rt)
-#pragma unroll
-          for (int i = 0; i < 4; ++i) {
-            int rloc = rt * 16 + q * 4 + i;
-#pragma unroll
-            for (int ct = 0; ct < 4; ++ct) {
-              int o = colb + ct * 16 + lm;
-              Fs[rloc][o] = elu(acc[rt][ct][i] + bo[o]);
-            }
-          }
-      }
-      __syncthreads();
-#pragma unroll
-      for (int j = 0; j < 4; ++j) {
-        int idx = j * 256 + t;
-        int rw = idx >> 5, cb4 = (idx & 31) * 4;
-        if (row0 + h2 * 32 + rw < N_NODES)
-          *(float4*)(fdst + (size_t)(row0 + h2 * 32 + rw) * HID + cb4) = *(const float4*)&Fs[rw][cb4];
-      }
-      __syncthreads();
-    }
-  }
+  const int NB = gridDim.x, bid = blockIdx.x;
+
+  for (int vb = bid; vb < VB_ZERO; vb += NB) phase_zero(a, vb, t);
+  if (bid == 0) phase_detect(a, t, (int*)smem_raw);
+  grid.sync();
+  for (int vb = bid; vb < VB_CVT; vb += NB) phase_cvt(a, vb, t);
+  grid.sync();
+  for (int vb = bid; vb < VB_SCAN; vb += NB) phase_scan1b(a, vb, t, lane, (int*)smem_raw);
+  grid.sync();
+  for (int vb = bid; vb < VB_PREP; vb += NB) phase_prep(a, vb, t, wave, lane, (int*)smem_raw);
+  grid.sync();
+  for (int vb = bid; vb < VB_SCAT; vb += NB) phase_scatter(a, vb, t);
+  grid.sync();
+  for (int vb = bid; vb < VB_ROWS; vb += NB) phase_l0(a, vb, t, wave, lane, lm, q, As, Cs);
+  grid.sync();
+  for (int vb = bid; vb < VB_EDGE; vb += NB) edge_vb(a, vb, (volatile float*)smem_raw, wave, lane);
+  grid.sync();
+  for (int vb = bid; vb < VB_ROWS; vb += NB) phase_mid(a, vb, t, wave, lane, lm, q, As, Cs);
+  grid.sync();
+  for (int vb = bid; vb < VB_EDGE; vb += NB) edge_vb(a, vb, (volatile float*)smem_raw, wave, lane);
+  grid.sync();
+  for (int vb = bid; vb < VB_ROWS; vb += NB) phase_final(a, vb, t, wave, lane, lm, q, As);
+}
+
+__global__ __launch_bounds__(256) void k_zero(MegaArgs a) {
+  __shared__ int dcnt[2];
+  phase_zero(a, blockIdx.x, threadIdx.x);
+  if (blockIdx.x == 0) phase_detect(a, threadIdx.x, dcnt);
+}
+__global__ __launch_bounds__(256) void k_cvt(MegaArgs a) {
+  phase_cvt(a, blockIdx.x, threadIdx.x);
+}
+__global__ __launch_bounds__(256) void k_scan1b(MegaArgs a) {
+  __shared__ int sm[256];
+  phase_scan1b(a, blockIdx.x, threadIdx.x, threadIdx.x & 63, sm);
+}
+__global__ __launch_bounds__(256) void k_prep(MegaArgs a) {
+  __shared__ int sm[256];
+  phase_prep(a, blockIdx.x, threadIdx.x, threadIdx.x >> 6, threadIdx.x & 63, sm);
+}
+__global__ __launch_bounds__(256) void k_scatter(MegaArgs a) {
+  phase_scatter(a, blockIdx.x, threadIdx.x);
+}
+__global__ __launch_bounds__(256) void k_l0(MegaArgs a) {
+  __shared__ unsigned short As[64][136];
+  __shared__ unsigned short Cs[64][136];
+  const int t = threadIdx.x, wave = t >> 6, lane = t & 63;
+  phase_l0(a, blockIdx.x, t, wave, lane, lane & 15, lane >> 4, As, Cs);
+}
+__global__ __launch_bounds__(256) void k_edge(MegaArgs a) {
+  __shared__ volatile float wbuf[1152];
+  phase_zero, (void)0;
+  edge_vb(a, blockIdx.x, wbuf, threadIdx.x >> 6, threadIdx.x & 63);
+}
+__global__ __launch_bounds__(256) void k_mid(MegaArgs a) {
+  __shared__ unsigned short As[64][136];
+  __shared__ unsigned short Cs[64][136];
+  const int t = threadIdx.x, wave = t >> 6, lane = t & 63;
+  phase_mid(a, blockIdx.x, t, wave, lane, lane & 15, lane >> 4, As, Cs);
+}
+__global__ __launch_bounds__(256) void k_final(MegaArgs a) {
+  __shared__ unsigned short As[64][136];
+  const int t = threadIdx.x, wave = t >> 6, lane = t & 63;
+  phase_final(a, blockIdx.x, t, wave, lane, lane & 15, lane >> 4, As);
 }
 
 extern "C" void kernel_launch(void* const* d_in, const int* in_sizes, int n_in,
                               void* d_out, int out_size, void* d_ws, size_t ws_size,
                               hipStream_t stream) {
-  const void* x     = d_in[0];
-  const int*  eidx  = (const int*)d_in[1];
-  const int*  etype = (const int*)d_in[2];
   const int iW[2] = {3, 9}, iQ[2] = {4, 10}, iK[2] = {5, 11}, icb[2] = {6, 12}, ipW[2] = {7, 13}, ipb[2] = {8, 14};
 
   float* ws = (float*)d_ws;
@@ -742,39 +772,52 @@
   float* pbf = ws + off; off += 2 * HID;
   float* bo2 = ws + off; off += 2 * HID;
 
-  detect_zero_kernel<<<(2 * NPAD + 16 + 255) / 256, 256, 0, stream>>>((const unsigned short*)x, eidx, flags, deg, 2 * NPAD + 16);
-
-  {
-    P8 tab;
-    float* base = ws;
-    for (int l = 0; l < 2; ++l) {
-      tab.src[l * 4 + 0] = d_in[iQ[l]];  tab.dstoff[l * 4 + 0] = (int)(Qf - base) + l * HID * HEADS;  tab.n[l * 4 + 0] = HID * HEADS;
-      tab.src[l * 4 + 1] = d_in[iK[l]];  tab.dstoff[l * 4 + 1] = (int)(Kf - base) + l * HID * HEADS;  tab.n[l * 4 + 1] = HID * HEADS;
-      tab.src[l * 4 + 2] = d_in[icb[l]]; tab.dstoff[l * 4 + 2] = (int)(cbf - base) + l * HID;         tab.n[l * 4 + 2] = HID;
-      tab.src[l * 4 + 3] = d_in[ipb[l]]; tab.dstoff[l * 4 + 3] = (int)(pbf - base) + l * HID;         tab.n[l * 4 + 3] = HID;
-    }
-    cvt_all_kernel<<<GB_IDX + GB_WT + 2, 256, 0, stream>>>(eidx, etype, dstA, pk, deg,
-                                                           d_in[iW[0]], d_in[iW[1]], Wbt,
-                                                           tab, ws, flags);
-  }
-
-  scan1_bucket_kernel<<<SCAN_B + SCAN_B, 256, 0, stream>>>(deg, excl, bsum, bcnt, nq, nwl);
-
-  scan23_prep_kernel<<<SCAN_B + 2 + 64, 256, 0, stream>>>(excl, bsum, rowstart,
-                                                          Wbt, Qf, Kf, qkt_hi, qkt_lo,
-                                                          d_in[ipW[0]], d_in[ipW[1]], cbf, pbf, pWTb2, bo2, flags);
-
-  scatter_kernel<<<(E_EDGES + 255) / 256, 256, 0, stream>>>(dstA, pk, rowstart, cnt, eord);
-
-  const int RB = NPAD / 64;
-  fused_l0_kernel<<<RB, 256, 0, stream>>>(x, Wbt, xw, qkt_hi, qkt_lo,
-                                          (float4*)qi, (float4*)kj, flags);
-  edge_all_kernel<<<GB_BIG + GB_QUAD, 256, 0, stream>>>(rowstart, eord, (const float4*)qi, (const float4*)kj,
-                                                        xw, aggb, nq, nwl, bcnt);
-  fused_mid_kernel<<<RB, 256, 0, stream>>>(aggb, pWTb2, bo2, Wbt + (size_t)2 * HID * HID, xw,
-                                           qkt_hi + (size_t)16 * HID, qkt_lo + (size_t)16 * HID,
-                                           (float4*)qi, (float4*)kj);
-  edge_all_kernel<<<GB_BIG + GB_QUAD, 256, 0, stream>>>(rowstart, eord, (const float4*)qi, (const float4*)kj,
-                                                        xw, aggb, nq, nwl, bcnt);
-  proj_final<<<RB, 256, 0, stream>>>(aggb, pWTb2 + (size_t)HID * HID, bo2 + HID, d_out, flags);
-}
+  MegaArgs a;
+  a.x = d_in[0]; a.eidx = (const int*)d_in[1]; a.etype = (const int*)d_in[2];
+  a.w0 = d_in[iW[0]]; a.w1 = d_in[iW[1]]; a.pW0 = d_in[ipW[0]]; a.pW1 = d_in[ipW[1]];
+  for (int l = 0; l < 2; ++l) {
+    a.tab.src[l * 4 + 0] = d_in[iQ[l]];  a.tab.dstoff[l * 4 + 0] = (int)(Qf - ws) + l * HID * HEADS;  a.tab.n[l * 4 + 0] = HID * HEADS;
+    a.tab.src[l * 4 + 1] = d_in[iK[l]];  a.tab.dstoff[l * 4 + 1] = (int)(Kf - ws) + l * HID * HEADS;  a.tab.n[l * 4 + 1] = HID * HEADS;
+    a.tab.src[l * 4 + 2] = d_in[icb[l]]; a.tab.dstoff[l * 4 + 2] = (int)(cbf - ws) + l * HID;         a.tab.n[l * 4 + 2] = HID;
+    a.tab.src[l * 4 + 3] = d_in[ipb[l]]; a.tab.dstoff[l * 4 + 3] = (int)(pbf - ws) + l * HID;         a.tab.n[l * 4 + 3] = HID;
+  }
+  a.base = ws;
+  a.flags = flags; a.xw = xw; a.qi4 = (float4*)qi; a.kj4 = (float4*)kj; a.aggb = aggb;
+  a.dstA = dstA; a.pk = pk; a.eord = eord; a.deg = deg; a.cnt = cnt; a.bcnt = bcnt;
+  a.excl = excl; a.rowstart = rowstart; a.bsum = bsum; a.nq = nq; a.nw = nwl;
+  a.Wbt = Wbt; a.pWTb2 = pWTb2; a.qkt_hi = qkt_hi; a.qkt_lo = qkt_lo;
+  a.Qf = Qf; a.Kf = Kf; a.cbf = cbf; a.pbf = pbf; a.bo2 = bo2;
+  a.dout = d_out;
+
+  static int s_cus = 0;
+  static int s_blocks_per_cu = -1;
+  if (s_blocks_per_cu == -1) {
+    hipDeviceProp_t prop;
+    if (hipGetDeviceProperties(&prop, 0) == hipSuccess && prop.multiProcessorCount > 0)
+      s_cus = prop.multiProcessorCount;
+    else
+      s_cus = 256;
+    int mb = 0;
+    if (hipOccupancyMaxActiveBlocksPerMultiprocessor(&mb, mega_kernel, 256, 0) != hipSuccess) mb = 0;
+    s_blocks_per_cu = (mb > 0) ? mb : 0;
+  }
+  if (s_blocks_per_cu > 0) {
+    int grid = s_blocks_per_cu * s_cus;
+    if (grid > 1024) grid = 1024;
+    void* kargs[] = { (void*)&a };
+    hipError_t e = hipLaunchCooperativeKernel(mega_kernel, dim3(grid), dim3(256), kargs, 0u, stream);
+    if (e == hipSuccess) return;
+    s_blocks_per_cu = 0;
+  }
+
+  k_zero<<<VB_ZERO, 256, 0, stream>>>(a);
+  k_cvt<<<VB_CVT, 256, 0, stream>>>(a);
+  k_scan1b<<<VB_SCAN, 256, 0, stream>>>(a);
+  k_prep<<<VB_PREP, 256, 0, stream>>>(a);
+  k_scatter<<<VB_SCAT, 256, 0, stream>>>(a);
+  k_l0<<<VB_ROWS, 256, 0, stream>>>(a);
+  k_edge<<<VB_EDGE, 256, 0, stream>>>(a);
+  k_mid<<<VB_ROWS, 256, 0, stream>>>(a);
+  k_edge<<<VB_EDGE, 256, 0, stream>>>(a);
+  k_final<<<VB_ROWS, 256, 0, stream>>>(a);
+}
```

Result: slower. 707.1 us (+106.1%).
